# Kernel optimization log

Measured on AMD Instinct MI355X. Metric: run time of the kernel, lower is better.

Reference implementation:

```python
import jax, jax.numpy as jnp
import numpy as np

BS, B, M, D, N = 8, 8, 512, 128, 1024
N_STEPS = 2
S_MAX = 3.0
BUDGET = 32.0
NEG = -1e30


def unit_normalize(x, eps=1e-12):
    return x / jnp.maximum(jnp.linalg.norm(x, axis=-1, keepdims=True), eps)


def setup_inputs() -> dict:
    key = jax.random.key(0)
    ks = jax.random.split(key, 10)
    return {
        "seed": jax.random.normal(ks[0], (BS, N, D), jnp.float32),
        "w_cand": jax.random.normal(ks[1], (BS, N, D), jnp.float32),
        "surprise": jax.random.normal(ks[2], (BS, N, D), jnp.float32),
        "g_em": jax.random.uniform(ks[3], (BS, B), jnp.float32),
        "em_K": unit_normalize(jax.random.normal(ks[4], (BS, B, M, D), jnp.float32)),
        "em_V": jax.random.normal(ks[5], (BS, B, M, D), jnp.float32),
        "em_S": jax.random.normal(ks[6], (BS, B, M), jnp.float32),  # ~half slots active (S>0)
        "em_age": jnp.zeros((BS, B, M), jnp.float32),
        "w1": 0.02 * jax.random.normal(ks[7], (B, D), jnp.float32),
        "w2": 0.02 * jax.random.normal(ks[8], (B, D), jnp.float32),
        "gate_bias": jnp.zeros((B, D), jnp.float32),
        "raw_tau": jnp.zeros((B,), jnp.float32),
        "raw_tau_w": jnp.zeros((B,), jnp.float32),
    }


def _masked_attn(scores, active, has_active):
    # scores: [BS,B,N,M]; active: [BS,B,1,M] bool; rows with no active slot -> 0 (nan_to_num(0))
    a = jax.nn.softmax(jnp.where(active, scores, NEG), axis=-1)
    return a * has_active


def reference(seed, w_cand, surprise, g_em, em_K, em_V, em_S, em_age,
              w1, w2, gate_bias, raw_tau, raw_tau_w):
    active = (em_S > 0.0)[:, :, None, :]                  # [BS,B,1,M]
    has_active = jnp.any(active, axis=-1, keepdims=True).astype(seed.dtype)

    # ---- trail_read_all (eval mode: no sigma noise) ----
    tau = (jax.nn.softplus(raw_tau) + 0.1)[None, :, None, None]
    s = jnp.broadcast_to(seed[:, None], (BS, B, N, D))
    y = s
    w1b, w2b, gbb = w1[None, :, None, :], w2[None, :, None, :], gate_bias[None, :, None, :]
    for _ in range(N_STEPS):
        scores = jnp.einsum('bknd,bkmd->bknm', y, em_K) / tau
        attn = _masked_attn(scores, active, has_active)
        delta = jnp.einsum('bknm,bkmd->bknd', attn, em_V)
        gate = jax.nn.sigmoid(w1b * y + w2b * delta + gbb)
        y = y + gate * delta
    y_em = jnp.transpose(y - s, (0, 2, 1, 3))             # [BS,N,B,D]

    # ---- compute_novelty_all (w_nov = None -> 0.5 blend) ----
    w_norm = unit_normalize(w_cand)[:, None]               # [BS,1,N,D]
    kT = jnp.swapaxes(em_K, -1, -2)                        # [BS,B,D,M]
    nov_scores = jnp.matmul(w_norm, kT) / tau              # [BS,B,N,M]
    nov_attn = _masked_attn(nov_scores, active, has_active)
    recon = jnp.matmul(nov_attn, em_V)                     # [BS,B,N,D]
    recon_err = jnp.linalg.norm(w_cand[:, None] - recon, axis=-1)   # [BS,B,N]
    surp_mag = jnp.linalg.norm(surprise, axis=-1)[:, None]          # [BS,1,N]
    novelty_bn = 0.5 * surp_mag + 0.5 * recon_err          # [BS,B,N]
    novelty = jnp.transpose(novelty_bn, (0, 2, 1))         # [BS,N,B]

    # ---- compute_write_deltas ----
    delta_em = novelty[..., None] * w_cand[:, :, None, :]  # [BS,N,B,D]

    # ---- commit_all ----
    tau_w = (jax.nn.softplus(raw_tau_w) + 0.1)[None, :, None, None]
    route_scores = jnp.matmul(w_norm, kT) / tau_w
    # all-inactive rows: softmax of all-equal NEG -> uniform 1/M == nan_to_num(1/M)
    route = jax.nn.softmax(jnp.where(active, route_scores, NEG), axis=-1)  # [BS,B,N,M]
    weighted_route = novelty_bn[..., None] * route          # [BS,B,N,M]
    route_agg = weighted_route.mean(axis=2)                 # [BS,B,M]
    wrT = jnp.swapaxes(weighted_route, 2, 3)                # [BS,B,M,N]
    update_K = jnp.matmul(wrT, w_norm)                      # [BS,B,M,D]
    update_V = jnp.matmul(wrT, w_cand[:, None])             # [BS,B,M,D]
    denom = jnp.maximum(weighted_route.sum(axis=2)[..., None], 1e-8)
    update_K = update_K / denom
    update_V = update_V / denom
    alpha = jnp.minimum(g_em[..., None] * route_agg, 1.0)   # [BS,B,M]
    ae = alpha[..., None]
    new_K = (1.0 - ae) * em_K + ae * unit_normalize(update_K)
    new_V = (1.0 - ae) * em_V + ae * update_V
    new_S = jnp.clip(em_S + alpha, 0.0, S_MAX)
    tot = new_S.sum(axis=-1, keepdims=True)                 # budget_enforce: scale sum to <= BUDGET
    new_S = new_S * jnp.minimum(1.0, BUDGET / jnp.maximum(tot, 1e-8))
    new_age = em_age * (1.0 - alpha)

    return (y_em, delta_em, new_K, new_V, new_S, new_age)
```

## Files before the change

kernel.cpp:

```cpp
#include <hip/hip_runtime.h>
#include <cstddef>

constexpr int BSz = 8;
constexpr int Bb  = 8;
constexpr int Mm  = 512;
constexpr int Dd  = 128;
constexpr int Nn  = 1024;
constexpr float NEGV = -1e30f;

typedef unsigned short ushort_t;
typedef __attribute__((ext_vector_type(8))) short short8v;
typedef __attribute__((ext_vector_type(4))) float f32x4;

__device__ __forceinline__ float softplusf(float x) {
    return (x > 20.f) ? x : log1pf(expf(x));
}
__device__ __forceinline__ unsigned short f2bf(float f) {
    unsigned u = __float_as_uint(f);
    u += 0x7fffu + ((u >> 16) & 1u);
    return (unsigned short)(u >> 16);
}
__device__ __forceinline__ unsigned pack2bf(float a, float b) {
    return (unsigned)f2bf(a) | ((unsigned)f2bf(b) << 16);
}
__device__ __forceinline__ f32x4 mfma16(short8v a, short8v b, f32x4 c) {
    return __builtin_amdgcn_mfma_f32_16x16x32_bf16(a, b, c, 0, 0, 0);
}

__device__ __forceinline__ void stage_K64(const float* __restrict__ src,
                                          ushort_t (*kl)[136], int tid) {
    const float4* s4 = (const float4*)src;
    #pragma unroll
    for (int it = 0; it < 8; ++it) {
        int i = tid + it * 256;
        int m = i >> 5, c = i & 31;
        float4 v = s4[i];
        uint2 w;
        w.x = pack2bf(v.x, v.y);
        w.y = pack2bf(v.z, v.w);
        *(uint2*)&kl[m][c * 4] = w;
    }
}

__device__ __forceinline__ void stage_VT(const float* __restrict__ src,
                                         ushort_t (*vt)[72], int tid) {
    const int wv = tid >> 6, l = tid & 63;
    const int c = l & 31, mh = l >> 5;
    #pragma unroll
    for (int it = 0; it < 8; ++it) {
        int pi = wv * 8 + it;
        int m0 = pi * 2;
        float4 mine = *(const float4*)(src + (size_t)(m0 + mh) * Dd + c * 4);
        float4 oth;
        oth.x = __shfl_xor(mine.x, 32);
        oth.y = __shfl_xor(mine.y, 32);
        oth.z = __shfl_xor(mine.z, 32);
        oth.w = __shfl_xor(mine.w, 32);
        float a0 = mh ? oth.z  : mine.x;
        float a1 = mh ? mine.z : oth.x;
        float b0 = mh ? oth.w  : mine.y;
        float b1 = mh ? mine.w : oth.y;
        int d0 = c * 4 + mh * 2;
        int sw = ((d0 >> 2) & 7) << 2;
        int col = m0 ^ sw;
        *(unsigned*)&vt[d0][col]     = pack2bf(a0, a1);
        *(unsigned*)&vt[d0 + 1][col] = pack2bf(b0, b1);
    }
}

__device__ __forceinline__ void stage_WVT(const float* __restrict__ src,
                                          const float* sinv,
                                          ushort_t (*vt)[72], int tid) {
    const int wv = tid >> 6, l = tid & 63;
    const int c = l & 31, mh = l >> 5;
    #pragma unroll
    for (int it = 0; it < 8; ++it) {
        int pi = wv * 8 + it;
        int m0 = pi * 2;
        float inv = sinv[m0 + mh];
        float4 mine = *(const float4*)(src + (size_t)(m0 + mh) * Dd + c * 4);
        mine.x *= inv; mine.y *= inv; mine.z *= inv; mine.w *= inv;
        float4 oth;
        oth.x = __shfl_xor(mine.x, 32);
        oth.y = __shfl_xor(mine.y, 32);
        oth.z = __shfl_xor(mine.z, 32);
        oth.w = __shfl_xor(mine.w, 32);
        float a0 = mh ? oth.z  : mine.x;
        float a1 = mh ? mine.z : oth.x;
        float b0 = mh ? oth.w  : mine.y;
        float b1 = mh ? mine.w : oth.y;
        int d0 = c * 4 + mh * 2;
        int sw = ((d0 >> 2) & 7) << 2;
        int col = m0 ^ sw;
        *(unsigned*)&vt[d0][col]     = pack2bf(a0, a1);
        *(unsigned*)&vt[d0 + 1][col] = pack2bf(b0, b1);
    }
}

__device__ __forceinline__ void transpose_yl_to_vt(const float (*yl)[132],
                                                   ushort_t (*vt)[72], int tid) {
    const int wv = tid >> 6, l = tid & 63;
    const int c = l & 31, mh = l >> 5;
    #pragma unroll
    for (int it = 0; it < 8; ++it) {
        int pi = wv * 8 + it;
        int m0 = pi * 2;
        float4 mine = *(const float4*)&yl[m0 + mh][c * 4];
        float4 oth;
        oth.x = __shfl_xor(mine.x, 32);
        oth.y = __shfl_xor(mine.y, 32);
        oth.z = __shfl_xor(mine.z, 32);
        oth.w = __shfl_xor(mine.w, 32);
        float a0 = mh ? oth.z  : mine.x;
        float a1 = mh ? mine.z : oth.x;
        float b0 = mh ? oth.w  : mine.y;
        float b1 = mh ? mine.w : oth.y;
        int d0 = c * 4 + mh * 2;
        int sw = ((d0 >> 2) & 7) << 2;
        int col = m0 ^ sw;
        *(unsigned*)&vt[d0][col]     = pack2bf(a0, a1);
        *(unsigned*)&vt[d0 + 1][col] = pack2bf(b0, b1);
    }
}

__device__ __forceinline__ short8v read_kfrag(const ushort_t (*kl)[136],
                                              int mt, int ck, int g, int q) {
    union { short8v s; uint4 u; } r;
    r.u = *(const uint4*)&kl[mt * 16 + q][ck * 32 + g * 8];
    return r.s;
}
__device__ __forceinline__ short8v build_yfrag(const float (*yl)[132], int row, int ck, int g) {
    float4 v0 = *(const float4*)&yl[row][ck * 32 + g * 8];
    float4 v1 = *(const float4*)&yl[row][ck * 32 + g * 8 + 4];
    union { short8v s; uint4 u; } r;
    r.u.x = pack2bf(v0.x, v0.y);
    r.u.y = pack2bf(v0.z, v0.w);
    r.u.z = pack2bf(v1.x, v1.y);
    r.u.w = pack2bf(v1.z, v1.w);
    return r.s;
}
__device__ __forceinline__ short8v read_vfrag(const ushort_t (*vt)[72],
                                              int kc, int dt, int g, int q) {
    int d = dt * 16 + q;
    int sw = ((d >> 2) & 7) << 2;
    uint2 lo = *(const uint2*)&vt[d][(kc * 32 + 4 * g) ^ sw];
    uint2 hi = *(const uint2*)&vt[d][(kc * 32 + 16 + 4 * g) ^ sw];
    union { short8v s; uint4 u; } r;
    r.u.x = lo.x; r.u.y = lo.y; r.u.z = hi.x; r.u.w = hi.y;
    return r.s;
}

__device__ __forceinline__ void kwrite(ushort_t (*kl)[136], const uint4* pf, int tid) {
    #pragma unroll
    for (int j = 0; j < 4; ++j) {
        int i = tid + j * 256;
        *(uint4*)&kl[i >> 4][(i & 15) * 8] = pf[j];
    }
}
__device__ __forceinline__ void vwrite(ushort_t (*vt)[72], const uint4* pf, int tid) {
    #pragma unroll
    for (int j = 0; j < 4; ++j) {
        int i = tid + j * 256;
        *(uint4*)&vt[i >> 3][(i & 7) * 8] = pf[j];
    }
}

__global__ __launch_bounds__(256) void k0kv(
    const float* __restrict__ emK, const float* __restrict__ emV,
    ushort_t* __restrict__ Kbf, ushort_t* __restrict__ Vtb)
{
    const int bs = blockIdx.z, b = blockIdx.y, mc = blockIdx.x;
    const int tid = threadIdx.x;
    const size_t pair = (size_t)(bs * Bb + b);
    __shared__ ushort_t vt[128][72];
    {
        const float4* s4 = (const float4*)(emK + (pair * Mm + (size_t)mc * 64) * Dd);
        uint2* dst = (uint2*)(Kbf + pair * 65536u + (size_t)mc * 8192u);
        #pragma unroll
        for (int it = 0; it < 8; ++it) {
            int i = tid + it * 256;
            float4 v = s4[i];
            uint2 w;
            w.x = pack2bf(v.x, v.y);
            w.y = pack2bf(v.z, v.w);
            dst[i] = w;
        }
    }
    stage_VT(emV + (pair * Mm + (size_t)mc * 64) * Dd, vt, tid);
    __syncthreads();
    {
        uint4* dst = (uint4*)(Vtb + pair * 65536u + (size_t)mc * 8192u);
        #pragma unroll
        for (int it = 0; it < 4; ++it) {
            int i = tid + it * 256;
            dst[i] = *(const uint4*)&vt[i >> 3][(i & 7) * 8];
        }
    }
}

__global__ __launch_bounds__(256) void k0w(
    const float* __restrict__ w_cand, ushort_t* __restrict__ wnr,
    ushort_t* __restrict__ wnT, float* __restrict__ nrmb)
{
    const int bs = blockIdx.y, nb = blockIdx.x * 64;
    const int tid = threadIdx.x;
    const int wv = tid >> 6, l = tid & 63, g = l >> 4, q = l & 15;
    __shared__ float yl[64][132];
    __shared__ ushort_t vt[128][72];
    {
        const float4* s4 = (const float4*)(w_cand + ((size_t)bs * Nn + nb) * Dd);
        #pragma unroll
        for (int it = 0; it < 8; ++it) {
            int i = tid + it * 256;
            *(float4*)&yl[i >> 5][(i & 31) * 4] = s4[i];
        }
    }
    __syncthreads();
    #pragma unroll
    for (int r = 0; r < 4; ++r) {
        int row = wv * 16 + 4 * g + r;
        float v8[8]; float p = 0.f;
        #pragma unroll
        for (int dt = 0; dt < 8; ++dt) { float v = yl[row][dt * 16 + q]; v8[dt] = v; p += v * v; }
        #pragma unroll
        for (int off = 1; off < 16; off <<= 1) p += __shfl_xor(p, off);
        float nrm = fmaxf(sqrtf(p), 1e-12f);
        float inv = 1.f / nrm;
        if (q == 0) nrmb[(size_t)bs * Nn + nb + row] = nrm;
        #pragma unroll
        for (int dt = 0; dt < 8; ++dt) yl[row][dt * 16 + q] = v8[dt] * inv;
    }
    __syncthreads();
    {
        uint4* dst = (uint4*)(wnr + (size_t)bs * 131072u) + (size_t)nb * 16u;
        #pragma unroll
        for (int j = 0; j < 4; ++j) {
            int i = tid + j * 256;
            int row = i >> 4, c8 = i & 15;
            float4 a = *(const float4*)&yl[row][c8 * 8];
            float4 c = *(const float4*)&yl[row][c8 * 8 + 4];
            uint4 w;
            w.x = pack2bf(a.x, a.y); w.y = pack2bf(a.z, a.w);
            w.z = pack2bf(c.x, c.y); w.w = pack2bf(c.z, c.w);
            dst[i] = w;
        }
    }
    transpose_yl_to_vt(yl, vt, tid);
    __syncthreads();
    {
        uint4* dst = (uint4*)(wnT + (size_t)bs * 131072u) + (size_t)(nb >> 6) * 1024u;
        #pragma unroll
        for (int it = 0; it < 4; ++it) {
            int i = tid + it * 256;
            dst[i] = *(const uint4*)&vt[i >> 3][(i & 7) * 8];
        }
    }
}

__global__ __launch_bounds__(256) void k1_pre(
    const float* __restrict__ seed, const ushort_t* __restrict__ Kbf,
    const ushort_t* __restrict__ Vtb, const float* __restrict__ emS,
    const float* __restrict__ w1, const float* __restrict__ w2,
    const float* __restrict__ gb, const float* __restrict__ rtau,
    float* __restrict__ y_em)
{
    const int bs = blockIdx.z, b = blockIdx.y, n0 = blockIdx.x * 64;
    const int tid = threadIdx.x;
    const int wv = tid >> 6, l = tid & 63, g = l >> 4, q = l & 15;

    __shared__ float yl[64][132];
    __shared__ ushort_t kl[64][136];
    __shared__ ushort_t vt[128][72];
    __shared__ float sw1[Dd], sw2[Dd], sgb[Dd];

    const float itau = 1.f / (softplusf(rtau[b]) + 0.1f);
    const size_t pair = (size_t)(bs * Bb + b);
    const uint4* Ksrc = (const uint4*)(Kbf + pair * 65536u);
    const uint4* Vsrc = (const uint4*)(Vtb + pair * 65536u);

    if (tid < Dd) {
        sw1[tid] = w1[b * Dd + tid];
        sw2[tid] = w2[b * Dd + tid];
        sgb[tid] = gb[b * Dd + tid];
    }
    unsigned long long mlo = 0ull, mhi = 0ull;
    {
        const float4* sp = (const float4*)(emS + pair * Mm);
        #pragma unroll 8
        for (int t = 0; t < 32; ++t) {
            float4 s = sp[t * 4 + g];
            unsigned long long bits = (s.x > 0.f ? 1ull : 0ull) | (s.y > 0.f ? 2ull : 0ull)
                                    | (s.z > 0.f ? 4ull : 0ull) | (s.w > 0.f ? 8ull : 0ull);
            if (t < 16) mlo |= bits << (t * 4);
            else        mhi |= bits << ((t - 16) * 4);
        }
    }
    {
        const float4* s4 = (const float4*)(seed + ((size_t)bs * Nn + n0) * Dd);
        #pragma unroll
        for (int it = 0; it < 8; ++it) {
            int i = tid + it * 256;
            *(float4*)&yl[i >> 5][(i & 31) * 4] = s4[i];
        }
    }
    uint4 kpf[4], vpf[4];
    #pragma unroll
    for (int j = 0; j < 4; ++j) { kpf[j] = Ksrc[tid + j * 256]; vpf[j] = Vsrc[tid + j * 256]; }
    __syncthreads();

    const f32x4 Z4 = {0.f, 0.f, 0.f, 0.f};

    for (int step = 0; step < 2; ++step) {
        short8v yf[4];
        #pragma unroll
        for (int ck = 0; ck < 4; ++ck) yf[ck] = build_yfrag(yl, wv * 16 + q, ck, g);

        float m_run = NEGV, l_run = 0.f;
        f32x4 dacc[8];
        #pragma unroll
        for (int dt = 0; dt < 8; ++dt) dacc[dt] = Z4;

        for (int mc = 0; mc < 8; ++mc) {
            kwrite(kl, kpf, tid);
            vwrite(vt, vpf, tid);
            __syncthreads();
            if (!(step == 1 && mc == 7)) {
                int nx = (mc < 7) ? mc + 1 : 0;
                #pragma unroll
                for (int j = 0; j < 4; ++j) {
                    kpf[j] = Ksrc[nx * 1024 + tid + j * 256];
                    vpf[j] = Vsrc[nx * 1024 + tid + j * 256];
                }
            }

            f32x4 sc[4];
            #pragma unroll
            for (int mt = 0; mt < 4; ++mt) {
                f32x4 acc = Z4;
                #pragma unroll
                for (int ck = 0; ck < 4; ++ck)
                    acc = mfma16(read_kfrag(kl, mt, ck, g, q), yf[ck], acc);
                sc[mt] = acc;
            }
            unsigned au = (unsigned)(((mc < 4) ? mlo : mhi) >> ((mc & 3) * 16)) & 0xFFFFu;
            #pragma unroll
            for (int mt = 0; mt < 4; ++mt)
                #pragma unroll
                for (int r = 0; r < 4; ++r)
                    sc[mt][r] = ((au >> (mt * 4 + r)) & 1u) ? sc[mt][r] * itau : NEGV;
            float cm = NEGV;
            #pragma unroll
            for (int mt = 0; mt < 4; ++mt)
                #pragma unroll
                for (int r = 0; r < 4; ++r) cm = fmaxf(cm, sc[mt][r]);
            cm = fmaxf(cm, __shfl_xor(cm, 16));
            cm = fmaxf(cm, __shfl_xor(cm, 32));
            float mnew = fmaxf(m_run, cm);
            float corr = __expf(m_run - mnew);
            unsigned pw[8];
            float psum = 0.f;
            #pragma unroll
            for (int mt = 0; mt < 4; ++mt)
                #pragma unroll
                for (int r = 0; r < 4; r += 2) {
                    float e0 = __expf(sc[mt][r]     - mnew);
                    float e1 = __expf(sc[mt][r + 1] - mnew);
                    psum += e0 + e1;
                    pw[mt * 2 + (r >> 1)] = pack2bf(e0, e1);
                }
            psum += __shfl_xor(psum, 16);
            psum += __shfl_xor(psum, 32);
            l_run = l_run * corr + psum;
            m_run = mnew;
            float cr[4];
            #pragma unroll
            for (int r = 0; r < 4; ++r) cr[r] = __shfl(corr, 4 * g + r);
            #pragma unroll
            for (int dt = 0; dt < 8; ++dt)
                #pragma unroll
                for (int r = 0; r < 4; ++r) dacc[dt][r] *= cr[r];
            union { short8v s; uint4 u; } pa0, pa1;
            pa0.u = make_uint4(pw[0], pw[1], pw[2], pw[3]);
            pa1.u = make_uint4(pw[4], pw[5], pw[6], pw[7]);
            #pragma unroll
            for (int dt = 0; dt < 8; ++dt) {
                f32x4 acc = dacc[dt];
                acc = mfma16(pa0.s, read_vfrag(vt, 0, dt, g, q), acc);
                acc = mfma16(pa1.s, read_vfrag(vt, 1, dt, g, q), acc);
                dacc[dt] = acc;
            }
            __syncthreads();
        }
        float inv = (m_run != NEGV) ? 1.f / l_run : 0.f;
        float ivr[4];
        #pragma unroll
        for (int r = 0; r < 4; ++r) ivr[r] = __shfl(inv, 4 * g + r);
        #pragma unroll
        for (int r = 0; r < 4; ++r) {
            int row = wv * 16 + 4 * g + r;
            #pragma unroll
            for (int dt = 0; dt < 8; ++dt) {
                int d = dt * 16 + q;
                float del = dacc[dt][r] * ivr[r];
                float y0 = yl[row][d];
                float z = sw1[d] * y0 + sw2[d] * del + sgb[d];
                float gte = 1.f / (1.f + __expf(-z));
                yl[row][d] = y0 + gte * del;
            }
        }
        __syncthreads();
    }
    #pragma unroll
    for (int r16 = 0; r16 < 16; ++r16) {
        int n = n0 + wv * 16 + r16;
        float2 sv = *(const float2*)(seed + ((size_t)bs * Nn + n) * Dd + 2 * l);
        float2 ov;
        ov.x = yl[wv * 16 + r16][2 * l]     - sv.x;
        ov.y = yl[wv * 16 + r16][2 * l + 1] - sv.y;
        *(float2*)(y_em + (((size_t)bs * Nn + n) * Bb + b) * Dd + 2 * l) = ov;
    }
}

__global__ __launch_bounds__(256) void k2a_pre(
    const float* __restrict__ w_cand, const float* __restrict__ surprise,
    const ushort_t* __restrict__ Kbf, const ushort_t* __restrict__ Vtb,
    const ushort_t* __restrict__ wnr, const float* __restrict__ emS,
    const float* __restrict__ rtau, const float* __restrict__ rtauw,
    float* __restrict__ delta_em, float* newV )
{
    const int bs = blockIdx.z, b = blockIdx.y, n0 = blockIdx.x * 64;
    const int tid = threadIdx.x;
    const int wv = tid >> 6, l = tid & 63, g = l >> 4, q = l & 15;

    __shared__ ushort_t kl[64][136];
    __shared__ ushort_t vt[128][72];

    const float itau = 1.f / (softplusf(rtau[b]) + 0.1f);
    const float itw  = 1.f / (softplusf(rtauw[b]) + 0.1f);
    const size_t pair = (size_t)(bs * Bb + b);
    const uint4* Ksrc = (const uint4*)(Kbf + pair * 65536u);
    const uint4* Vsrc = (const uint4*)(Vtb + pair * 65536u);
    float* stats = newV + pair * (size_t)(Mm * Dd) + 448 * Dd;

    unsigned long long mlo = 0ull, mhi = 0ull;
    {
        const float4* sp = (const float4*)(emS + pair * Mm);
        #pragma unroll 8
        for (int t = 0; t < 32; ++t) {
            float4 s = sp[t * 4 + g];
            unsigned long long bits = (s.x > 0.f ? 1ull : 0ull) | (s.y > 0.f ? 2ull : 0ull)
                                    | (s.z > 0.f ? 4ull : 0ull) | (s.w > 0.f ? 8ull : 0ull);
            if (t < 16) mlo |= bits << (t * 4);
            else        mhi |= bits << ((t - 16) * 4);
        }
    }
    short8v yf[4];
    {
        const uint4* wr = (const uint4*)(wnr + (size_t)bs * 131072u
                                         + (size_t)(n0 + wv * 16 + q) * 128u);
        #pragma unroll
        for (int ck = 0; ck < 4; ++ck) {
            union { short8v s; uint4 u; } r;
            r.u = wr[ck * 4 + g];
            yf[ck] = r.s;
        }
    }
    uint4 kpf[4], vpf[4];
    #pragma unroll
    for (int j = 0; j < 4; ++j) { kpf[j] = Ksrc[tid + j * 256]; vpf[j] = Vsrc[tid + j * 256]; }

    const f32x4 Z4 = {0.f, 0.f, 0.f, 0.f};
    float m1 = NEGV, l1 = 0.f, m2 = NEGV, s2 = 0.f;
    f32x4 dacc[8];
    #pragma unroll
    for (int dt = 0; dt < 8; ++dt) dacc[dt] = Z4;

    for (int mc = 0; mc < 8; ++mc) {
        kwrite(kl, kpf, tid);
        vwrite(vt, vpf, tid);
        __syncthreads();
        if (mc < 7) {
            #pragma unroll
            for (int j = 0; j < 4; ++j) {
                kpf[j] = Ksrc[(mc + 1) * 1024 + tid + j * 256];
                vpf[j] = Vsrc[(mc + 1) * 1024 + tid + j * 256];
            }
        }

        f32x4 sc[4];
        #pragma unroll
        for (int mt = 0; mt < 4; ++mt) {
            f32x4 acc = Z4;
            #pragma unroll
            for (int ck = 0; ck < 4; ++ck)
                acc = mfma16(read_kfrag(kl, mt, ck, g, q), yf[ck], acc);
            sc[mt] = acc;
        }
        unsigned au = (unsigned)(((mc < 4) ? mlo : mhi) >> ((mc & 3) * 16)) & 0xFFFFu;

        float cm2 = NEGV;
        #pragma unroll
        for (int mt = 0; mt < 4; ++mt)
            #pragma unroll
            for (int r = 0; r < 4; ++r) {
                float v = ((au >> (mt * 4 + r)) & 1u) ? sc[mt][r] * itw : NEGV;
                cm2 = fmaxf(cm2, v);
            }
        cm2 = fmaxf(cm2, __shfl_xor(cm2, 16));
        cm2 = fmaxf(cm2, __shfl_xor(cm2, 32));
        float mn2 = fmaxf(m2, cm2);
        float c2 = __expf(m2 - mn2);
        float ps2 = 0.f;
        #pragma unroll
        for (int mt = 0; mt < 4; ++mt)
            #pragma unroll
            for (int r = 0; r < 4; ++r) {
                float v = ((au >> (mt * 4 + r)) & 1u) ? sc[mt][r] * itw : NEGV;
                ps2 += __expf(v - mn2);
            }
        ps2 += __shfl_xor(ps2, 16);
        ps2 += __shfl_xor(ps2, 32);
        s2 = s2 * c2 + ps2;
        m2 = mn2;

        #pragma unroll
        for (int mt = 0; mt < 4; ++mt)
            #pragma unroll
            for (int r = 0; r < 4; ++r)
                sc[mt][r] = ((au >> (mt * 4 + r)) & 1u) ? sc[mt][r] * itau : NEGV;
        float cm = NEGV;
        #pragma unroll
        for (int mt = 0; mt < 4; ++mt)
            #pragma unroll
            for (int r = 0; r < 4; ++r) cm = fmaxf(cm, sc[mt][r]);
        cm = fmaxf(cm, __shfl_xor(cm, 16));
        cm = fmaxf(cm, __shfl_xor(cm, 32));
        float mnew = fmaxf(m1, cm);
        float corr = __expf(m1 - mnew);
        unsigned pw[8];
        float psum = 0.f;
        #pragma unroll
        for (int mt = 0; mt < 4; ++mt)
            #pragma unroll
            for (int r = 0; r < 4; r += 2) {
                float e0 = __expf(sc[mt][r]     - mnew);
                float e1 = __expf(sc[mt][r + 1] - mnew);
                psum += e0 + e1;
                pw[mt * 2 + (r >> 1)] = pack2bf(e0, e1);
            }
        psum += __shfl_xor(psum, 16);
        psum += __shfl_xor(psum, 32);
        l1 = l1 * corr + psum;
        m1 = mnew;
        float cr[4];
        #pragma unroll
        for (int r = 0; r < 4; ++r) cr[r] = __shfl(corr, 4 * g + r);
        #pragma unroll
        for (int dt = 0; dt < 8; ++dt)
            #pragma unroll
            for (int r = 0; r < 4; ++r) dacc[dt][r] *= cr[r];
        union { short8v s; uint4 u; } pa0, pa1;
        pa0.u = make_uint4(pw[0], pw[1], pw[2], pw[3]);
        pa1.u = make_uint4(pw[4], pw[5], pw[6], pw[7]);
        #pragma unroll
        for (int dt = 0; dt < 8; ++dt) {
            f32x4 acc = dacc[dt];
            acc = mfma16(pa0.s, read_vfrag(vt, 0, dt, g, q), acc);
            acc = mfma16(pa1.s, read_vfrag(vt, 1, dt, g, q), acc);
            dacc[dt] = acc;
        }
        __syncthreads();
    }
    if (g == 0) {
        int n = n0 + wv * 16 + q;
        stats[1024 + n] = m2;
        stats[2048 + n] = s2;
    }
    float inv1 = (m1 != NEGV) ? 1.f / l1 : 0.f;
    float ivr[4];
    #pragma unroll
    for (int r = 0; r < 4; ++r) ivr[r] = __shfl(inv1, 4 * g + r);
    #pragma unroll
    for (int r = 0; r < 4; ++r) {
        int n = n0 + wv * 16 + 4 * g + r;
        const float* wcr = w_cand + ((size_t)bs * Nn + n) * Dd;
        const float* spr = surprise + ((size_t)bs * Nn + n) * Dd;
        float pe = 0.f, ps = 0.f, wcv[8];
        #pragma unroll
        for (int dt = 0; dt < 8; ++dt) {
            float wc = wcr[dt * 16 + q];
            float rec = dacc[dt][r] * ivr[r];
            float df = wc - rec;
            pe += df * df;
            float sv = spr[dt * 16 + q];
            ps += sv * sv;
            wcv[dt] = wc;
        }
        #pragma unroll
        for (int off = 1; off < 16; off <<= 1) {
            pe += __shfl_xor(pe, off);
            ps += __shfl_xor(ps, off);
        }
        float novl = 0.5f * sqrtf(ps) + 0.5f * sqrtf(pe);
        if (q == 0) stats[n] = novl;
        float* der = delta_em + (((size_t)bs * Nn + n) * Bb + b) * Dd;
        #pragma unroll
        for (int dt = 0; dt < 8; ++dt) der[dt * 16 + q] = novl * wcv[dt];
    }
}

__global__ __launch_bounds__(256) void k2b_pre(
    const ushort_t* __restrict__ wnr, const ushort_t* __restrict__ wnT,
    const ushort_t* __restrict__ Kbf,
    const float* __restrict__ emK, const float* __restrict__ emV,
    const float* __restrict__ emS, const float* __restrict__ emAge,
    const float* __restrict__ g_em, const float* __restrict__ rtauw,
    const float* __restrict__ nrmb,
    float* __restrict__ newK, float* newV ,
    float* __restrict__ newAge, float* __restrict__ newS, int mt_base)
{
    const int bs = blockIdx.z, b = blockIdx.y, mt = mt_base + blockIdx.x;
    const int m0 = mt * 64;
    const int tid = threadIdx.x;
    const int wv = tid >> 6, l = tid & 63, g = l >> 4, q = l & 15;

    __shared__ ushort_t klw[64][136];
    __shared__ ushort_t vtw[128][72];
    __shared__ float sh_rm[Nn], sh_f[Nn], sh_fn[Nn];

    const float itw = 1.f / (softplusf(rtauw[b]) + 0.1f);
    const float gv = g_em[bs * Bb + b];
    const size_t pair = (size_t)(bs * Bb + b);
    const float* stats = newV + pair * (size_t)(Mm * Dd) + 448 * Dd;

    for (int i = tid; i < Nn; i += 256) {
        float nv = stats[i];
        float rm = stats[1024 + i];
        float rs = stats[2048 + i];
        float nr = nrmb[(size_t)bs * Nn + i];
        sh_rm[i] = rm;
        float f = nv / rs;
        sh_f[i]  = f;
        sh_fn[i] = f * nr;
    }

    const int myM = m0 + wv * 16 + q;
    short8v kf[4];
    {
        const uint4* kr = (const uint4*)(Kbf + pair * 65536u + (size_t)myM * 128u);
        #pragma unroll
        for (int ck = 0; ck < 4; ++ck) {
            union { short8v s; uint4 u; } r;
            r.u = kr[ck * 4 + g];
            kf[ck] = r.s;
        }
    }
    const bool act = (emS[pair * Mm + myM] > 0.f);

    const uint4* Wr = (const uint4*)(wnr + (size_t)bs * 131072u);
    const uint4* Wt = (const uint4*)(wnT + (size_t)bs * 131072u);
    uint4 wpf[4], tpf[4];
    #pragma unroll
    for (int j = 0; j < 4; ++j) { wpf[j] = Wr[tid + j * 256]; tpf[j] = Wt[tid + j * 256]; }

    const f32x4 Z4 = {0.f, 0.f, 0.f, 0.f};
    f32x4 uKacc[8], uVacc[8];
    #pragma unroll
    for (int dt = 0; dt < 8; ++dt) { uKacc[dt] = Z4; uVacc[dt] = Z4; }
    float den = 0.f;

    for (int nc = 0; nc < 16; ++nc) {
        const int nb = nc * 64;
        kwrite(klw, wpf, tid);
        vwrite(vtw, tpf, tid);
        __syncthreads();
        if (nc < 15) {
            #pragma unroll
            for (int j = 0; j < 4; ++j) {
                wpf[j] = Wr[(nc + 1) * 1024 + tid + j * 256];
                tpf[j] = Wt[(nc + 1) * 1024 + tid + j * 256];
            }
        }

        f32x4 sc[4];
        #pragma unroll
        for (int nt = 0; nt < 4; ++nt) {
            f32x4 acc = Z4;
            #pragma unroll
            for (int ck = 0; ck < 4; ++ck)
                acc = mfma16(read_kfrag(klw, nt, ck, g, q), kf[ck], acc);
            sc[nt] = acc;
        }
        unsigned pwK[8], pwV[8];
        #pragma unroll
        for (int nt = 0; nt < 4; ++nt) {
            float w0[4], w1[4];
            #pragma unroll
            for (int r = 0; r < 4; ++r) {
                int nl = nb + nt * 16 + 4 * g + r;
                float val = act ? sc[nt][r] * itw : NEGV;
                float E = __expf(val - sh_rm[nl]);
                float a = sh_f[nl] * E;
                w0[r] = a;
                w1[r] = sh_fn[nl] * E;
                den += a;
            }
            pwK[nt * 2 + 0] = pack2bf(w0[0], w0[1]);
            pwK[nt * 2 + 1] = pack2bf(w0[2], w0[3]);
            pwV[nt * 2 + 0] = pack2bf(w1[0], w1[1]);
            pwV[nt * 2 + 1] = pack2bf(w1[2], w1[3]);
        }
        union { short8v s; uint4 u; } paK0, paK1, paV0, paV1;
        paK0.u = make_uint4(pwK[0], pwK[1], pwK[2], pwK[3]);
        paK1.u = make_uint4(pwK[4], pwK[5], pwK[6], pwK[7]);
        paV0.u = make_uint4(pwV[0], pwV[1], pwV[2], pwV[3]);
        paV1.u = make_uint4(pwV[4], pwV[5], pwV[6], pwV[7]);
        #pragma unroll
        for (int dt = 0; dt < 8; ++dt) {
            short8v b0 = read_vfrag(vtw, 0, dt, g, q);
            short8v b1 = read_vfrag(vtw, 1, dt, g, q);
            uKacc[dt] = mfma16(paK0.s, b0, uKacc[dt]);
            uKacc[dt] = mfma16(paK1.s, b1, uKacc[dt]);
            uVacc[dt] = mfma16(paV0.s, b0, uVacc[dt]);
            uVacc[dt] = mfma16(paV1.s, b1, uVacc[dt]);
        }
        __syncthreads();
    }

    den += __shfl_xor(den, 16);
    den += __shfl_xor(den, 32);
    float invd = 1.f / fmaxf(den, 1e-8f);
    float alpha = fminf(gv * den * (1.f / (float)Nn), 1.f);

    float pr[4] = {0.f, 0.f, 0.f, 0.f};
    #pragma unroll
    for (int dt = 0; dt < 8; ++dt)
        #pragma unroll
        for (int r = 0; r < 4; ++r) { float u = uKacc[dt][r]; pr[r] += u * u; }
    #pragma unroll
    for (int r = 0; r < 4; ++r) {
        #pragma unroll
        for (int off = 1; off < 16; off <<= 1) pr[r] += __shfl_xor(pr[r], off);
    }
    float alr[4], idr[4], inr[4];
    #pragma unroll
    for (int r = 0; r < 4; ++r) {
        alr[r] = __shfl(alpha, 4 * g + r);
        idr[r] = __shfl(invd,  4 * g + r);
        inr[r] = 1.f / fmaxf(sqrtf(pr[r]) * idr[r], 1e-12f);
    }
    #pragma unroll
    for (int r = 0; r < 4; ++r) {
        size_t rowoff = (pair * Mm + m0 + wv * 16 + 4 * g + r) * (size_t)Dd;
        float a = alr[r], om = 1.f - a, id = idr[r], in = inr[r];
        #pragma unroll
        for (int dt = 0; dt < 8; ++dt) {
            int d = dt * 16 + q;
            float kv = emK[rowoff + d];
            float vv = emV[rowoff + d];
            newK[rowoff + d] = om * kv + a * uKacc[dt][r] * id * in;
            newV[rowoff + d] = om * vv + a * uVacc[dt][r] * id;
        }
    }
    if (q == 0) {
        #pragma unroll
        for (int r = 0; r < 4; ++r) {
            int m = m0 + wv * 16 + 4 * g + r;
            float a = alr[r];
            float S = emS[pair * Mm + m];
            newS[pair * Mm + m] = fminf(fmaxf(S + a, 0.f), 3.0f);
            newAge[pair * Mm + m] = emAge[pair * Mm + m] * (1.f - a);
        }
    }
}

__global__ __launch_bounds__(256) void k1_fb(
    const float* __restrict__ seed, const float* __restrict__ emK, const float* __restrict__ emV,
    const float* __restrict__ emS, const float* __restrict__ w1, const float* __restrict__ w2,
    const float* __restrict__ gb, const float* __restrict__ rtau, float* __restrict__ y_em)
{
    const int bs = blockIdx.z, b = blockIdx.y, n0 = blockIdx.x * 64;
    const int tid = threadIdx.x;
    const int wv = tid >> 6, l = tid & 63, g = l >> 4, q = l & 15;

    __shared__ float yl[64][132];
    __shared__ ushort_t kl[64][136];
    __shared__ ushort_t vt[128][72];
    __shared__ float sw1[Dd], sw2[Dd], sgb[Dd];

    const float itau = 1.f / (softplusf(rtau[b]) + 0.1f);
    const size_t pair = (size_t)(bs * Bb + b);
    const float* Kb = emK + pair * (size_t)(Mm * Dd);
    const float* Vb = emV + pair * (size_t)(Mm * Dd);

    if (tid < Dd) {
        sw1[tid] = w1[b * Dd + tid];
        sw2[tid] = w2[b * Dd + tid];
        sgb[tid] = gb[b * Dd + tid];
    }
    unsigned long long mlo = 0ull, mhi = 0ull;
    {
        const float4* sp = (const float4*)(emS + pair * Mm);
        #pragma unroll 8
        for (int t = 0; t < 32; ++t) {
            float4 s = sp[t * 4 + g];
            unsigned long long bits = (s.x > 0.f ? 1ull : 0ull) | (s.y > 0.f ? 2ull : 0ull)
                                    | (s.z > 0.f ? 4ull : 0ull) | (s.w > 0.f ? 8ull : 0ull);
            if (t < 16) mlo |= bits << (t * 4);
            else        mhi |= bits << ((t - 16) * 4);
        }
    }
    {
        const float4* s4 = (const float4*)(seed + ((size_t)bs * Nn + n0) * Dd);
        #pragma unroll
        for (int it = 0; it < 8; ++it) {
            int i = tid + it * 256;
            *(float4*)&yl[i >> 5][(i & 31) * 4] = s4[i];
        }
    }
    __syncthreads();

    const f32x4 Z4 = {0.f, 0.f, 0.f, 0.f};

    for (int step = 0; step < 2; ++step) {
        short8v yf[4];
        #pragma unroll
        for (int ck = 0; ck < 4; ++ck) yf[ck] = build_yfrag(yl, wv * 16 + q, ck, g);

        float m_run = NEGV, l_run = 0.f;
        f32x4 dacc[8];
        #pragma unroll
        for (int dt = 0; dt < 8; ++dt) dacc[dt] = Z4;

        for (int mc = 0; mc < 8; ++mc) {
            stage_K64(Kb + (size_t)mc * 64 * Dd, kl, tid);
            stage_VT(Vb + (size_t)mc * 64 * Dd, vt, tid);
            __syncthreads();

            f32x4 sc[4];
            #pragma unroll
            for (int mt = 0; mt < 4; ++mt) {
                f32x4 acc = Z4;
                #pragma unroll
                for (int ck = 0; ck < 4; ++ck)
                    acc = mfma16(read_kfrag(kl, mt, ck, g, q), yf[ck], acc);
                sc[mt] = acc;
            }
            unsigned au = (unsigned)(((mc < 4) ? mlo : mhi) >> ((mc & 3) * 16)) & 0xFFFFu;
            #pragma unroll
            for (int mt = 0; mt < 4; ++mt)
                #pragma unroll
                for (int r = 0; r < 4; ++r)
                    sc[mt][r] = ((au >> (mt * 4 + r)) & 1u) ? sc[mt][r] * itau : NEGV;
            float cm = NEGV;
            #pragma unroll
            for (int mt = 0; mt < 4; ++mt)
                #pragma unroll
                for (int r = 0; r < 4; ++r) cm = fmaxf(cm, sc[mt][r]);
            cm = fmaxf(cm, __shfl_xor(cm, 16));
            cm = fmaxf(cm, __shfl_xor(cm, 32));
            float mnew = fmaxf(m_run, cm);
            float corr = __expf(m_run - mnew);
            unsigned pw[8];
            float psum = 0.f;
            #pragma unroll
            for (int mt = 0; mt < 4; ++mt)
                #pragma unroll
                for (int r = 0; r < 4; r += 2) {
                    float e0 = __expf(sc[mt][r]     - mnew);
                    float e1 = __expf(sc[mt][r + 1] - mnew);
                    psum += e0 + e1;
                    pw[mt * 2 + (r >> 1)] = pack2bf(e0, e1);
                }
            psum += __shfl_xor(psum, 16);
            psum += __shfl_xor(psum, 32);
            l_run = l_run * corr + psum;
            m_run = mnew;
            float cr[4];
            #pragma unroll
            for (int r = 0; r < 4; ++r) cr[r] = __shfl(corr, 4 * g + r);
            #pragma unroll
            for (int dt = 0; dt < 8; ++dt)
                #pragma unroll
                for (int r = 0; r < 4; ++r) dacc[dt][r] *= cr[r];
            union { short8v s; uint4 u; } pa0, pa1;
            pa0.u = make_uint4(pw[0], pw[1], pw[2], pw[3]);
            pa1.u = make_uint4(pw[4], pw[5], pw[6], pw[7]);
            #pragma unroll
            for (int dt = 0; dt < 8; ++dt) {
                f32x4 acc = dacc[dt];
                acc = mfma16(pa0.s, read_vfrag(vt, 0, dt, g, q), acc);
                acc = mfma16(pa1.s, read_vfrag(vt, 1, dt, g, q), acc);
                dacc[dt] = acc;
            }
            __syncthreads();
        }
        float inv = (m_run != NEGV) ? 1.f / l_run : 0.f;
        float ivr[4];
        #pragma unroll
        for (int r = 0; r < 4; ++r) ivr[r] = __shfl(inv, 4 * g + r);
        #pragma unroll
        for (int r = 0; r < 4; ++r) {
            int row = wv * 16 + 4 * g + r;
            #pragma unroll
            for (int dt = 0; dt < 8; ++dt) {
                int d = dt * 16 + q;
                float del = dacc[dt][r] * ivr[r];
                float y0 = yl[row][d];
                float z = sw1[d] * y0 + sw2[d] * del + sgb[d];
                float gte = 1.f / (1.f + __expf(-z));
                yl[row][d] = y0 + gte * del;
            }
        }
        __syncthreads();
    }
    #pragma unroll
    for (int r16 = 0; r16 < 16; ++r16) {
        int n = n0 + wv * 16 + r16;
        float2 sv = *(const float2*)(seed + ((size_t)bs * Nn + n) * Dd + 2 * l);
        float2 ov;
        ov.x = yl[wv * 16 + r16][2 * l]     - sv.x;
        ov.y = yl[wv * 16 + r16][2 * l + 1] - sv.y;
        *(float2*)(y_em + (((size_t)bs * Nn + n) * Bb + b) * Dd + 2 * l) = ov;
    }
}

__global__ __launch_bounds__(256) void k2a_fb(
    const float* __restrict__ w_cand, const float* __restrict__ surprise,
    const float* __restrict__ emK, const float* __restrict__ emV, const float* __restrict__ emS,
    const float* __restrict__ rtau, const float* __restrict__ rtauw,
    float* __restrict__ delta_em, float* newV)
{
    const int bs = blockIdx.z, b = blockIdx.y, n0 = blockIdx.x * 64;
    const int tid = threadIdx.x;
    const int wv = tid >> 6, l = tid & 63, g = l >> 4, q = l & 15;

    __shared__ float yl[64][132];
    __shared__ ushort_t kl[64][136];
    __shared__ ushort_t vt[128][72];

    const float itau = 1.f / (softplusf(rtau[b]) + 0.1f);
    const float itw  = 1.f / (softplusf(rtauw[b]) + 0.1f);
    const size_t pair = (size_t)(bs * Bb + b);
    const float* Kb = emK + pair * (size_t)(Mm * Dd);
    const float* Vb = emV + pair * (size_t)(Mm * Dd);
    float* stats = newV + pair * (size_t)(Mm * Dd) + 448 * Dd;

    unsigned long long mlo = 0ull, mhi = 0ull;
    {
        const float4* sp = (const float4*)(emS + pair * Mm);
        #pragma unroll 8
        for (int t = 0; t < 32; ++t) {
            float4 s = sp[t * 4 + g];
            unsigned long long bits = (s.x > 0.f ? 1ull : 0ull) | (s.y > 0.f ? 2ull : 0ull)
                                    | (s.z > 0.f ? 4ull : 0ull) | (s.w > 0.f ? 8ull : 0ull);
            if (t < 16) mlo |= bits << (t * 4);
            else        mhi |= bits << ((t - 16) * 4);
        }
    }
    {
        const float4* s4 = (const float4*)(w_cand + ((size_t)bs * Nn + n0) * Dd);
        #pragma unroll
        for (int it = 0; it < 8; ++it) {
            int i = tid + it * 256;
            *(float4*)&yl[i >> 5][(i & 31) * 4] = s4[i];
        }
    }
    __syncthreads();
    #pragma unroll
    for (int r = 0; r < 4; ++r) {
        int row = wv * 16 + 4 * g + r;
        float v8[8]; float p = 0.f;
        #pragma unroll
        for (int dt = 0; dt < 8; ++dt) { float v = yl[row][dt * 16 + q]; v8[dt] = v; p += v * v; }
        #pragma unroll
        for (int off = 1; off < 16; off <<= 1) p += __shfl_xor(p, off);
        float nrm = fmaxf(sqrtf(p), 1e-12f);
        float invn = 1.f / nrm;
        if (q == 0) stats[3072 + n0 + row] = nrm;
        #pragma unroll
        for (int dt = 0; dt < 8; ++dt) yl[row][dt * 16 + q] = v8[dt] * invn;
    }
    __syncthreads();

    const f32x4 Z4 = {0.f, 0.f, 0.f, 0.f};
    short8v yf[4];
    #pragma unroll
    for (int ck = 0; ck < 4; ++ck) yf[ck] = build_yfrag(yl, wv * 16 + q, ck, g);

    float m1 = NEGV, l1 = 0.f, m2 = NEGV, s2 = 0.f;
    f32x4 dacc[8];
    #pragma unroll
    for (int dt = 0; dt < 8; ++dt) dacc[dt] = Z4;

    for (int mc = 0; mc < 8; ++mc) {
        stage_K64(Kb + (size_t)mc * 64 * Dd, kl, tid);
        stage_VT(Vb + (size_t)mc * 64 * Dd, vt, tid);
        __syncthreads();

        f32x4 sc[4];
        #pragma unroll
        for (int mt = 0; mt < 4; ++mt) {
            f32x4 acc = Z4;
            #pragma unroll
            for (int ck = 0; ck < 4; ++ck)
                acc = mfma16(read_kfrag(kl, mt, ck, g, q), yf[ck], acc);
            sc[mt] = acc;
        }
        unsigned au = (unsigned)(((mc < 4) ? mlo : mhi) >> ((mc & 3) * 16)) & 0xFFFFu;

        float cm2 = NEGV;
        #pragma unroll
        for (int mt = 0; mt < 4; ++mt)
            #pragma unroll
            for (int r = 0; r < 4; ++r) {
                float v = ((au >> (mt * 4 + r)) & 1u) ? sc[mt][r] * itw : NEGV;
                cm2 = fmaxf(cm2, v);
            }
        cm2 = fmaxf(cm2, __shfl_xor(cm2, 16));
        cm2 = fmaxf(cm2, __shfl_xor(cm2, 32));
        float mn2 = fmaxf(m2, cm2);
        float c2 = __expf(m2 - mn2);
        float ps2 = 0.f;
        #pragma unroll
        for (int mt = 0; mt < 4; ++mt)
            #pragma unroll
            for (int r = 0; r < 4; ++r) {
                float v = ((au >> (mt * 4 + r)) & 1u) ? sc[mt][r] * itw : NEGV;
                ps2 += __expf(v - mn2);
            }
        ps2 += __shfl_xor(ps2, 16);
        ps2 += __shfl_xor(ps2, 32);
        s2 = s2 * c2 + ps2;
        m2 = mn2;

        #pragma unroll
        for (int mt = 0; mt < 4; ++mt)
            #pragma unroll
            for (int r = 0; r < 4; ++r)
                sc[mt][r] = ((au >> (mt * 4 + r)) & 1u) ? sc[mt][r] * itau : NEGV;
        float cm = NEGV;
        #pragma unroll
        for (int mt = 0; mt < 4; ++mt)
            #pragma unroll
            for (int r = 0; r < 4; ++r) cm = fmaxf(cm, sc[mt][r]);
        cm = fmaxf(cm, __shfl_xor(cm, 16));
        cm = fmaxf(cm, __shfl_xor(cm, 32));
        float mnew = fmaxf(m1, cm);
        float corr = __expf(m1 - mnew);
        unsigned pw[8];
        float psum = 0.f;
        #pragma unroll
        for (int mt = 0; mt < 4; ++mt)
            #pragma unroll
            for (int r = 0; r < 4; r += 2) {
                float e0 = __expf(sc[mt][r]     - mnew);
                float e1 = __expf(sc[mt][r + 1] - mnew);
                psum += e0 + e1;
                pw[mt * 2 + (r >> 1)] = pack2bf(e0, e1);
            }
        psum += __shfl_xor(psum, 16);
        psum += __shfl_xor(psum, 32);
        l1 = l1 * corr + psum;
        m1 = mnew;
        float cr[4];
        #pragma unroll
        for (int r = 0; r < 4; ++r) cr[r] = __shfl(corr, 4 * g + r);
        #pragma unroll
        for (int dt = 0; dt < 8; ++dt)
            #pragma unroll
            for (int r = 0; r < 4; ++r) dacc[dt][r] *= cr[r];
        union { short8v s; uint4 u; } pa0, pa1;
        pa0.u = make_uint4(pw[0], pw[1], pw[2], pw[3]);
        pa1.u = make_uint4(pw[4], pw[5], pw[6], pw[7]);
        #pragma unroll
        for (int dt = 0; dt < 8; ++dt) {
            f32x4 acc = dacc[dt];
            acc = mfma16(pa0.s, read_vfrag(vt, 0, dt, g, q), acc);
            acc = mfma16(pa1.s, read_vfrag(vt, 1, dt, g, q), acc);
            dacc[dt] = acc;
        }
        __syncthreads();
    }
    if (g == 0) {
        int n = n0 + wv * 16 + q;
        stats[1024 + n] = m2;
        stats[2048 + n] = s2;
    }
    float inv1 = (m1 != NEGV) ? 1.f / l1 : 0.f;
    float ivr[4];
    #pragma unroll
    for (int r = 0; r < 4; ++r) ivr[r] = __shfl(inv1, 4 * g + r);
    #pragma unroll
    for (int r = 0; r < 4; ++r) {
        int n = n0 + wv * 16 + 4 * g + r;
        const float* wcr = w_cand + ((size_t)bs * Nn + n) * Dd;
        const float* spr = surprise + ((size_t)bs * Nn + n) * Dd;
        float pe = 0.f, ps = 0.f, wcv[8];
        #pragma unroll
        for (int dt = 0; dt < 8; ++dt) {
            float wc = wcr[dt * 16 + q];
            float rec = dacc[dt][r] * ivr[r];
            float df = wc - rec;
            pe += df * df;
            float sv = spr[dt * 16 + q];
            ps += sv * sv;
            wcv[dt] = wc;
        }
        #pragma unroll
        for (int off = 1; off < 16; off <<= 1) {
            pe += __shfl_xor(pe, off);
            ps += __shfl_xor(ps, off);
        }
        float novl = 0.5f * sqrtf(ps) + 0.5f * sqrtf(pe);
        if (q == 0) stats[n] = novl;
        float* der = delta_em + (((size_t)bs * Nn + n) * Bb + b) * Dd;
        #pragma unroll
        for (int dt = 0; dt < 8; ++dt) der[dt * 16 + q] = novl * wcv[dt];
    }
}

__global__ __launch_bounds__(256) void k2b_fb(
    const float* __restrict__ w_cand, const float* __restrict__ emK, const float* __restrict__ emV,
    const float* __restrict__ emS, const float* __restrict__ emAge,
    const float* __restrict__ g_em, const float* __restrict__ rtauw,
    float* __restrict__ newK, float* newV,
    float* __restrict__ newAge, float* __restrict__ newS, int mt_base)
{
    const int bs = blockIdx.z, b = blockIdx.y, mt = mt_base + blockIdx.x;
    const int m0 = mt * 64;
    const int tid = threadIdx.x;
    const int wv = tid >> 6, l = tid & 63, g = l >> 4, q = l & 15;

    __shared__ ushort_t klw[64][136];
    __shared__ ushort_t vtw[128][72];
    __shared__ float sh_rm[Nn], sh_f[Nn], sh_fn[Nn], sh_inv[Nn];

    const float itw = 1.f / (softplusf(rtauw[b]) + 0.1f);
    const float gv = g_em[bs * Bb + b];
    const size_t pair = (size_t)(bs * Bb + b);
    const float* stats = newV + pair * (size_t)(Mm * Dd) + 448 * Dd;

    for (int i = tid; i < Nn; i += 256) {
        float nv = stats[i];
        float rm = stats[1024 + i];
        float rs = stats[2048 + i];
        float nr = stats[3072 + i];
        sh_rm[i] = rm;
        float f = nv / rs;
        sh_f[i]  = f;
        sh_fn[i] = f * nr;
        sh_inv[i] = 1.f / nr;
    }

    const int myM = m0 + wv * 16 + q;
    const float* Krow = emK + (pair * Mm + myM) * (size_t)Dd;
    short8v kf[4];
    #pragma unroll
    for (int ck = 0; ck < 4; ++ck) {
        float4 a = *(const float4*)(Krow + ck * 32 + g * 8);
        float4 c = *(const float4*)(Krow + ck * 32 + g * 8 + 4);
        union { short8v s; uint4 u; } r;
        r.u.x = pack2bf(a.x, a.y);
        r.u.y = pack2bf(a.z, a.w);
        r.u.z = pack2bf(c.x, c.y);
        r.u.w = pack2bf(c.z, c.w);
        kf[ck] = r.s;
    }
    const bool act = (emS[pair * Mm + myM] > 0.f);

    const f32x4 Z4 = {0.f, 0.f, 0.f, 0.f};
    f32x4 uKacc[8], uVacc[8];
    #pragma unroll
    for (int dt = 0; dt < 8; ++dt) { uKacc[dt] = Z4; uVacc[dt] = Z4; }
    float den = 0.f;

    __syncthreads();

    for (int nc = 0; nc < 16; ++nc) {
        const int nb = nc * 64;
        if (nc) __syncthreads();
        {
            const float4* s4 = (const float4*)(w_cand + ((size_t)bs * Nn + nb) * Dd);
            #pragma unroll
            for (int it = 0; it < 8; ++it) {
                int i = tid + it * 256;
                int m = i >> 5, c = i & 31;
                float4 v = s4[i];
                float inv = sh_inv[nb + m];
                uint2 w;
                w.x = pack2bf(v.x * inv, v.y * inv);
                w.y = pack2bf(v.z * inv, v.w * inv);
                *(uint2*)&klw[m][c * 4] = w;
            }
        }
        stage_WVT(w_cand + ((size_t)bs * Nn + nb) * Dd, sh_inv + nb, vtw, tid);
        __syncthreads();

        f32x4 sc[4];
        #pragma unroll
        for (int nt = 0; nt < 4; ++nt) {
            f32x4 acc = Z4;
            #pragma unroll
            for (int ck = 0; ck < 4; ++ck)
                acc = mfma16(read_kfrag(klw, nt, ck, g, q), kf[ck], acc);
            sc[nt] = acc;
        }
        unsigned pwK[8], pwV[8];
        #pragma unroll
        for (int nt = 0; nt < 4; ++nt) {
            float w0[4], w1[4];
            #pragma unroll
            for (int r = 0; r < 4; ++r) {
                int nl = nb + nt * 16 + 4 * g + r;
                float val = act ? sc[nt][r] * itw : NEGV;
                float E = __expf(val - sh_rm[nl]);
                float a = sh_f[nl] * E;
                w0[r] = a;
                w1[r] = sh_fn[nl] * E;
                den += a;
            }
            pwK[nt * 2 + 0] = pack2bf(w0[0], w0[1]);
            pwK[nt * 2 + 1] = pack2bf(w0[2], w0[3]);
            pwV[nt * 2 + 0] = pack2bf(w1[0], w1[1]);
            pwV[nt * 2 + 1] = pack2bf(w1[2], w1[3]);
        }
        union { short8v s; uint4 u; } paK0, paK1, paV0, paV1;
        paK0.u = make_uint4(pwK[0], pwK[1], pwK[2], pwK[3]);
        paK1.u = make_uint4(pwK[4], pwK[5], pwK[6], pwK[7]);
        paV0.u = make_uint4(pwV[0], pwV[1], pwV[2], pwV[3]);
        paV1.u = make_uint4(pwV[4], pwV[5], pwV[6], pwV[7]);
        #pragma unroll
        for (int dt = 0; dt < 8; ++dt) {
            short8v b0 = read_vfrag(vtw, 0, dt, g, q);
            short8v b1 = read_vfrag(vtw, 1, dt, g, q);
            uKacc[dt] = mfma16(paK0.s, b0, uKacc[dt]);
            uKacc[dt] = mfma16(paK1.s, b1, uKacc[dt]);
            uVacc[dt] = mfma16(paV0.s, b0, uVacc[dt]);
            uVacc[dt] = mfma16(paV1.s, b1, uVacc[dt]);
        }
    }

    den += __shfl_xor(den, 16);
    den += __shfl_xor(den, 32);
    float invd = 1.f / fmaxf(den, 1e-8f);
    float alpha = fminf(gv * den * (1.f / (float)Nn), 1.f);

    float pr[4] = {0.f, 0.f, 0.f, 0.f};
    #pragma unroll
    for (int dt = 0; dt < 8; ++dt)
        #pragma unroll
        for (int r = 0; r < 4; ++r) { float u = uKacc[dt][r]; pr[r] += u * u; }
    #pragma unroll
    for (int r = 0; r < 4; ++r) {
        #pragma unroll
        for (int off = 1; off < 16; off <<= 1) pr[r] += __shfl_xor(pr[r], off);
    }
    float alr[4], idr[4], inr[4];
    #pragma unroll
    for (int r = 0; r < 4; ++r) {
        alr[r] = __shfl(alpha, 4 * g + r);
        idr[r] = __shfl(invd,  4 * g + r);
        inr[r] = 1.f / fmaxf(sqrtf(pr[r]) * idr[r], 1e-12f);
    }
    #pragma unroll
    for (int r = 0; r < 4; ++r) {
        size_t rowoff = (pair * Mm + m0 + wv * 16 + 4 * g + r) * (size_t)Dd;
        float a = alr[r], om = 1.f - a, id = idr[r], in = inr[r];
        #pragma unroll
        for (int dt = 0; dt < 8; ++dt) {
            int d = dt * 16 + q;
            float kv = emK[rowoff + d];
            float vv = emV[rowoff + d];
            newK[rowoff + d] = om * kv + a * uKacc[dt][r] * id * in;
            newV[rowoff + d] = om * vv + a * uVacc[dt][r] * id;
        }
    }
    if (q == 0) {
        #pragma unroll
        for (int r = 0; r < 4; ++r) {
            int m = m0 + wv * 16 + 4 * g + r;
            float a = alr[r];
            float S = emS[pair * Mm + m];
            newS[pair * Mm + m] = fminf(fmaxf(S + a, 0.f), 3.0f);
            newAge[pair * Mm + m] = emAge[pair * Mm + m] * (1.f - a);
        }
    }
}

__global__ __launch_bounds__(256) void k2c_scale(float* newS)
{
    const int p = blockIdx.x, tid = threadIdx.x;
    __shared__ float red[256];
    float v0 = newS[(size_t)p * Mm + tid];
    float v1 = newS[(size_t)p * Mm + 256 + tid];
    red[tid] = v0 + v1;
    __syncthreads();
    for (int s = 128; s > 0; s >>= 1) {
        if (tid < s) red[tid] += red[tid + s];
        __syncthreads();
    }
    float tot = red[0];
    float sc = fminf(1.f, 32.0f / fmaxf(tot, 1e-8f));
    newS[(size_t)p * Mm + tid]       = v0 * sc;
    newS[(size_t)p * Mm + 256 + tid] = v1 * sc;
}

extern "C" void kernel_launch(void* const* d_in, const int* in_sizes, int n_in,
                              void* d_out, int out_size, void* d_ws, size_t ws_size,
                              hipStream_t stream)
{
    const float* seed     = (const float*)d_in[0];
    const float* w_cand   = (const float*)d_in[1];
    const float* surprise = (const float*)d_in[2];
    const float* g_em     = (const float*)d_in[3];
    const float* emK      = (const float*)d_in[4];
    const float* emV      = (const float*)d_in[5];
    const float* emS      = (const float*)d_in[6];
    const float* emAge    = (const float*)d_in[7];
    const float* w1       = (const float*)d_in[8];
    const float* w2       = (const float*)d_in[9];
    const float* gb       = (const float*)d_in[10];
    const float* rtau     = (const float*)d_in[11];
    const float* rtauw    = (const float*)d_in[12];

    float* out = (float*)d_out;
    float* y_em     = out;
    float* delta_em = out + (size_t)8388608;
    float* newK     = out + (size_t)16777216;
    float* newV     = out + (size_t)20971520;
    float* newS     = out + (size_t)25165824;
    float* newAge   = out + (size_t)25198592;

    dim3 blk(256);
    dim3 g1(Nn / 64, Bb, BSz);

    const size_t WS_NEED = 21004288;
    if (d_ws != nullptr && ws_size >= WS_NEED) {
        ushort_t* Kbf = (ushort_t*)d_ws;
        ushort_t* Vtb = Kbf + (size_t)64 * 65536;
        ushort_t* wnr = Vtb + (size_t)64 * 65536;
        ushort_t* wnT = wnr + (size_t)8 * 131072;
        float*    nrmb = (float*)(wnT + (size_t)8 * 131072);

        k0kv<<<dim3(8, Bb, BSz), blk, 0, stream>>>(emK, emV, Kbf, Vtb);
        k0w<<<dim3(16, BSz), blk, 0, stream>>>(w_cand, wnr, wnT, nrmb);
        k1_pre<<<g1, blk, 0, stream>>>(seed, Kbf, Vtb, emS, w1, w2, gb, rtau, y_em);
        k2a_pre<<<g1, blk, 0, stream>>>(w_cand, surprise, Kbf, Vtb, wnr, emS,
                                        rtau, rtauw, delta_em, newV);
        k2b_pre<<<dim3(7, Bb, BSz), blk, 0, stream>>>(wnr, wnT, Kbf, emK, emV, emS, emAge,
                                                      g_em, rtauw, nrmb,
                                                      newK, newV, newAge, newS, 0);
        k2b_pre<<<dim3(1, Bb, BSz), blk, 0, stream>>>(wnr, wnT, Kbf, emK, emV, emS, emAge,
                                                      g_em, rtauw, nrmb,
                                                      newK, newV, newAge, newS, 7);
    } else {
        k1_fb<<<g1, blk, 0, stream>>>(seed, emK, emV, emS, w1, w2, gb, rtau, y_em);
        k2a_fb<<<g1, blk, 0, stream>>>(w_cand, surprise, emK, emV, emS, rtau, rtauw,
                                       delta_em, newV);
        k2b_fb<<<dim3(7, Bb, BSz), blk, 0, stream>>>(w_cand, emK, emV, emS, emAge, g_em, rtauw,
                                                     newK, newV, newAge, newS, 0);
        k2b_fb<<<dim3(1, Bb, BSz), blk, 0, stream>>>(w_cand, emK, emV, emS, emAge, g_em, rtauw,
                                                     newK, newV, newAge, newS, 7);
    }
    k2c_scale<<<dim3(64), blk, 0, stream>>>(newS);
}
```

Before: 695.9 us.

## Split trail-read steps into separate launches and remap blocks to 1D grids

The fused two-step k1_pre kernel becomes k1_step, launched once per step. The intermediate y is stored to y_em in global memory rather than kept in LDS, and the y fragment is built straight from global memory. All kernels now use 1D grids with the batch index b (or bs) in the low bits, so blocks sharing the same K/V or w_cand data run close together and may hit in cache. This drops the 64x132 float LDS buffer, which can raise occupancy, but it adds an extra launch and a global round trip of y.

New measurement: 712.4 us. +2.4%, slower.

```diff
diff --git a/kernel.cpp b/kernel.cpp
--- a/kernel.cpp
+++ b/kernel.cpp
@@ -139,6 +139,16 @@
     r.u.w = pack2bf(v1.z, v1.w);
     return r.s;
 }
+__device__ __forceinline__ short8v build_gfrag(const float* __restrict__ yr, int ck, int g) {
+    float4 a = *(const float4*)(yr + ck * 32 + g * 8);
+    float4 c = *(const float4*)(yr + ck * 32 + g * 8 + 4);
+    union { short8v s; uint4 u; } r;
+    r.u.x = pack2bf(a.x, a.y);
+    r.u.y = pack2bf(a.z, a.w);
+    r.u.z = pack2bf(c.x, c.y);
+    r.u.w = pack2bf(c.z, c.w);
+    return r.s;
+}
 __device__ __forceinline__ short8v read_vfrag(const ushort_t (*vt)[72],
                                               int kc, int dt, int g, int q) {
     int d = dt * 16 + q;
@@ -165,11 +175,27 @@
     }
 }
 
+__device__ __forceinline__ void build_mask(const float* __restrict__ emS, size_t pair,
+                                           int g, unsigned long long& mlo,
+                                           unsigned long long& mhi) {
+    mlo = 0ull; mhi = 0ull;
+    const float4* sp = (const float4*)(emS + pair * Mm);
+    #pragma unroll 8
+    for (int t = 0; t < 32; ++t) {
+        float4 s = sp[t * 4 + g];
+        unsigned long long bits = (s.x > 0.f ? 1ull : 0ull) | (s.y > 0.f ? 2ull : 0ull)
+                                | (s.z > 0.f ? 4ull : 0ull) | (s.w > 0.f ? 8ull : 0ull);
+        if (t < 16) mlo |= bits << (t * 4);
+        else        mhi |= bits << ((t - 16) * 4);
+    }
+}
+
 __global__ __launch_bounds__(256) void k0kv(
     const float* __restrict__ emK, const float* __restrict__ emV,
     ushort_t* __restrict__ Kbf, ushort_t* __restrict__ Vtb)
 {
-    const int bs = blockIdx.z, b = blockIdx.y, mc = blockIdx.x;
+    const int id = blockIdx.x;
+    const int b = id & 7, t = id >> 3, mc = t & 7, bs = t >> 3;
     const int tid = threadIdx.x;
     const size_t pair = (size_t)(bs * Bb + b);
     __shared__ ushort_t vt[128][72];
@@ -202,7 +228,8 @@
     const float* __restrict__ w_cand, ushort_t* __restrict__ wnr,
     ushort_t* __restrict__ wnT, float* __restrict__ nrmb)
 {
-    const int bs = blockIdx.y, nb = blockIdx.x * 64;
+    const int id = blockIdx.x;
+    const int bs = id & 7, nb = (id >> 3) * 64;
     const int tid = threadIdx.x;
     const int wv = tid >> 6, l = tid & 63, g = l >> 4, q = l & 15;
     __shared__ float yl[64][132];
@@ -257,12 +284,500 @@
     }
 }
 
-__global__ __launch_bounds__(256) void k1_pre(
+__global__ __launch_bounds__(256) void k1_step(
     const float* __restrict__ seed, const ushort_t* __restrict__ Kbf,
     const ushort_t* __restrict__ Vtb, const float* __restrict__ emS,
     const float* __restrict__ w1, const float* __restrict__ w2,
     const float* __restrict__ gb, const float* __restrict__ rtau,
-    float* __restrict__ y_em)
+    float* __restrict__ y_em, int step)
+{
+    const int id = blockIdx.x;
+    const int b = id & 7, bs = id >> 7, n0 = ((id >> 3) & 15) << 6;
+    const int tid = threadIdx.x;
+    const int wv = tid >> 6, l = tid & 63, g = l >> 4, q = l & 15;
+
+    __shared__ ushort_t kl[64][136];
+    __shared__ ushort_t vt[128][72];
+    __shared__ float sw1[Dd], sw2[Dd], sgb[Dd];
+
+    const float itau = 1.f / (softplusf(rtau[b]) + 0.1f);
+    const size_t pair = (size_t)(bs * Bb + b);
+    const uint4* Ksrc = (const uint4*)(Kbf + pair * 65536u);
+    const uint4* Vsrc = (const uint4*)(Vtb + pair * 65536u);
+
+    if (tid < Dd) {
+        sw1[tid] = w1[b * Dd + tid];
+        sw2[tid] = w2[b * Dd + tid];
+        sgb[tid] = gb[b * Dd + tid];
+    }
+    unsigned long long mlo, mhi;
+    build_mask(emS, pair, g, mlo, mhi);
+
+    short8v yf[4];
+    {
+        int n = n0 + wv * 16 + q;
+        const float* yr = step ? (y_em + (((size_t)bs * Nn + n) * Bb + b) * Dd)
+                               : (seed + ((size_t)bs * Nn + n) * Dd);
+        #pragma unroll
+        for (int ck = 0; ck < 4; ++ck) yf[ck] = build_gfrag(yr, ck, g);
+    }
+    uint4 kpf[4], vpf[4];
+    #pragma unroll
+    for (int j = 0; j < 4; ++j) { kpf[j] = Ksrc[tid + j * 256]; vpf[j] = Vsrc[tid + j * 256]; }
+
+    const f32x4 Z4 = {0.f, 0.f, 0.f, 0.f};
+    float m_run = NEGV, l_run = 0.f;
+    f32x4 dacc[8];
+    #pragma unroll
+    for (int dt = 0; dt < 8; ++dt) dacc[dt] = Z4;
+
+    for (int mc = 0; mc < 8; ++mc) {
+        kwrite(kl, kpf, tid);
+        vwrite(vt, vpf, tid);
+        __syncthreads();
+        if (mc < 7) {
+            #pragma unroll
+            for (int j = 0; j < 4; ++j) {
+                kpf[j] = Ksrc[(mc + 1) * 1024 + tid + j * 256];
+                vpf[j] = Vsrc[(mc + 1) * 1024 + tid + j * 256];
+            }
+        }
+
+        f32x4 sc[4];
+        #pragma unroll
+        for (int mt = 0; mt < 4; ++mt) {
+            f32x4 acc = Z4;
+            #pragma unroll
+            for (int ck = 0; ck < 4; ++ck)
+                acc = mfma16(read_kfrag(kl, mt, ck, g, q), yf[ck], acc);
+            sc[mt] = acc;
+        }
+        unsigned au = (unsigned)(((mc < 4) ? mlo : mhi) >> ((mc & 3) * 16)) & 0xFFFFu;
+        #pragma unroll
+        for (int mt = 0; mt < 4; ++mt)
+            #pragma unroll
+            for (int r = 0; r < 4; ++r)
+                sc[mt][r] = ((au >> (mt * 4 + r)) & 1u) ? sc[mt][r] * itau : NEGV;
+        float cm = NEGV;
+        #pragma unroll
+        for (int mt = 0; mt < 4; ++mt)
+            #pragma unroll
+            for (int r = 0; r < 4; ++r) cm = fmaxf(cm, sc[mt][r]);
+        cm = fmaxf(cm, __shfl_xor(cm, 16));
+        cm = fmaxf(cm, __shfl_xor(cm, 32));
+        float mnew = fmaxf(m_run, cm);
+        float corr = __expf(m_run - mnew);
+        unsigned pw[8];
+        float psum = 0.f;
+        #pragma unroll
+        for (int mt = 0; mt < 4; ++mt)
+            #pragma unroll
+            for (int r = 0; r < 4; r += 2) {
+                float e0 = __expf(sc[mt][r]     - mnew);
+                float e1 = __expf(sc[mt][r + 1] - mnew);
+                psum += e0 + e1;
+                pw[mt * 2 + (r >> 1)] = pack2bf(e0, e1);
+            }
+        psum += __shfl_xor(psum, 16);
+        psum += __shfl_xor(psum, 32);
+        l_run = l_run * corr + psum;
+        m_run = mnew;
+        float cr[4];
+        #pragma unroll
+        for (int r = 0; r < 4; ++r) cr[r] = __shfl(corr, 4 * g + r);
+        #pragma unroll
+        for (int dt = 0; dt < 8; ++dt)
+            #pragma unroll
+            for (int r = 0; r < 4; ++r) dacc[dt][r] *= cr[r];
+        union { short8v s; uint4 u; } pa0, pa1;
+        pa0.u = make_uint4(pw[0], pw[1], pw[2], pw[3]);
+        pa1.u = make_uint4(pw[4], pw[5], pw[6], pw[7]);
+        #pragma unroll
+        for (int dt = 0; dt < 8; ++dt) {
+            f32x4 acc = dacc[dt];
+            acc = mfma16(pa0.s, read_vfrag(vt, 0, dt, g, q), acc);
+            acc = mfma16(pa1.s, read_vfrag(vt, 1, dt, g, q), acc);
+            dacc[dt] = acc;
+        }
+        __syncthreads();
+    }
+    float inv = (m_run != NEGV) ? 1.f / l_run : 0.f;
+    float ivr[4];
+    #pragma unroll
+    for (int r = 0; r < 4; ++r) ivr[r] = __shfl(inv, 4 * g + r);
+    #pragma unroll
+    for (int r = 0; r < 4; ++r) {
+        int n = n0 + wv * 16 + 4 * g + r;
+        const float* yr = step ? (y_em + (((size_t)bs * Nn + n) * Bb + b) * Dd)
+                               : (seed + ((size_t)bs * Nn + n) * Dd);
+        const float* sr = seed + ((size_t)bs * Nn + n) * Dd;
+        float* yo = y_em + (((size_t)bs * Nn + n) * Bb + b) * Dd;
+        #pragma unroll
+        for (int dt = 0; dt < 8; ++dt) {
+            int d = dt * 16 + q;
+            float y0 = yr[d];
+            float del = dacc[dt][r] * ivr[r];
+            float z = sw1[d] * y0 + sw2[d] * del + sgb[d];
+            float gte = 1.f / (1.f + __expf(-z));
+            float yn = y0 + gte * del;
+            yo[d] = step ? (yn - sr[d]) : yn;
+        }
+    }
+}
+
+__global__ __launch_bounds__(256) void k2a_pre(
+    const float* __restrict__ w_cand, const float* __restrict__ surprise,
+    const ushort_t* __restrict__ Kbf, const ushort_t* __restrict__ Vtb,
+    const ushort_t* __restrict__ wnr, const float* __restrict__ emS,
+    const float* __restrict__ rtau, const float* __restrict__ rtauw,
+    float* __restrict__ delta_em, float* newV )
+{
+    const int id = blockIdx.x;
+    const int b = id & 7, bs = id >> 7, n0 = ((id >> 3) & 15) << 6;
+    const int tid = threadIdx.x;
+    const int wv = tid >> 6, l = tid & 63, g = l >> 4, q = l & 15;
+
+    __shared__ ushort_t kl[64][136];
+    __shared__ ushort_t vt[128][72];
+
+    const float itau = 1.f / (softplusf(rtau[b]) + 0.1f);
+    const float itw  = 1.f / (softplusf(rtauw[b]) + 0.1f);
+    const size_t pair = (size_t)(bs * Bb + b);
+    const uint4* Ksrc = (const uint4*)(Kbf + pair * 65536u);
+    const uint4* Vsrc = (const uint4*)(Vtb + pair * 65536u);
+    float* stats = newV + pair * (size_t)(Mm * Dd) + 448 * Dd;
+
+    unsigned long long mlo, mhi;
+    build_mask(emS, pair, g, mlo, mhi);
+
+    short8v yf[4];
+    {
+        const uint4* wr = (const uint4*)(wnr + (size_t)bs * 131072u
+                                         + (size_t)(n0 + wv * 16 + q) * 128u);
+        #pragma unroll
+        for (int ck = 0; ck < 4; ++ck) {
+            union { short8v s; uint4 u; } r;
+            r.u = wr[ck * 4 + g];
+            yf[ck] = r.s;
+        }
+    }
+    uint4 kpf[4], vpf[4];
+    #pragma unroll
+    for (int j = 0; j < 4; ++j) { kpf[j] = Ksrc[tid + j * 256]; vpf[j] = Vsrc[tid + j * 256]; }
+
+    const f32x4 Z4 = {0.f, 0.f, 0.f, 0.f};
+    float m1 = NEGV, l1 = 0.f, m2 = NEGV, s2 = 0.f;
+    f32x4 dacc[8];
+    #pragma unroll
+    for (int dt = 0; dt < 8; ++dt) dacc[dt] = Z4;
+
+    for (int mc = 0; mc < 8; ++mc) {
+        kwrite(kl, kpf, tid);
+        vwrite(vt, vpf, tid);
+        __syncthreads();
+        if (mc < 7) {
+            #pragma unroll
+            for (int j = 0; j < 4; ++j) {
+                kpf[j] = Ksrc[(mc + 1) * 1024 + tid + j * 256];
+                vpf[j] = Vsrc[(mc + 1) * 1024 + tid + j * 256];
+            }
+        }
+
+        f32x4 sc[4];
+        #pragma unroll
+        for (int mt = 0; mt < 4; ++mt) {
+            f32x4 acc = Z4;
+            #pragma unroll
+            for (int ck = 0; ck < 4; ++ck)
+                acc = mfma16(read_kfrag(kl, mt, ck, g, q), yf[ck], acc);
+            sc[mt] = acc;
+        }
+        unsigned au = (unsigned)(((mc < 4) ? mlo : mhi) >> ((mc & 3) * 16)) & 0xFFFFu;
+
+        float cm2 = NEGV;
+        #pragma unroll
+        for (int mt = 0; mt < 4; ++mt)
+            #pragma unroll
+            for (int r = 0; r < 4; ++r) {
+                float v = ((au >> (mt * 4 + r)) & 1u) ? sc[mt][r] * itw : NEGV;
+                cm2 = fmaxf(cm2, v);
+            }
+        cm2 = fmaxf(cm2, __shfl_xor(cm2, 16));
+        cm2 = fmaxf(cm2, __shfl_xor(cm2, 32));
+        float mn2 = fmaxf(m2, cm2);
+        float c2 = __expf(m2 - mn2);
+        float ps2 = 0.f;
+        #pragma unroll
+        for (int mt = 0; mt < 4; ++mt)
+            #pragma unroll
+            for (int r = 0; r < 4; ++r) {
+                float v = ((au >> (mt * 4 + r)) & 1u) ? sc[mt][r] * itw : NEGV;
+                ps2 += __expf(v - mn2);
+            }
+        ps2 += __shfl_xor(ps2, 16);
+        ps2 += __shfl_xor(ps2, 32);
+        s2 = s2 * c2 + ps2;
+        m2 = mn2;
+
+        #pragma unroll
+        for (int mt = 0; mt < 4; ++mt)
+            #pragma unroll
+            for (int r = 0; r < 4; ++r)
+                sc[mt][r] = ((au >> (mt * 4 + r)) & 1u) ? sc[mt][r] * itau : NEGV;
+        float cm = NEGV;
+        #pragma unroll
+        for (int mt = 0; mt < 4; ++mt)
+            #pragma unroll
+            for (int r = 0; r < 4; ++r) cm = fmaxf(cm, sc[mt][r]);
+        cm = fmaxf(cm, __shfl_xor(cm, 16));
+        cm = fmaxf(cm, __shfl_xor(cm, 32));
+        float mnew = fmaxf(m1, cm);
+        float corr = __expf(m1 - mnew);
+        unsigned pw[8];
+        float psum = 0.f;
+        #pragma unroll
+        for (int mt = 0; mt < 4; ++mt)
+            #pragma unroll
+            for (int r = 0; r < 4; r += 2) {
+                float e0 = __expf(sc[mt][r]     - mnew);
+                float e1 = __expf(sc[mt][r + 1] - mnew);
+                psum += e0 + e1;
+                pw[mt * 2 + (r >> 1)] = pack2bf(e0, e1);
+            }
+        psum += __shfl_xor(psum, 16);
+        psum += __shfl_xor(psum, 32);
+        l1 = l1 * corr + psum;
+        m1 = mnew;
+        float cr[4];
+        #pragma unroll
+        for (int r = 0; r < 4; ++r) cr[r] = __shfl(corr, 4 * g + r);
+        #pragma unroll
+        for (int dt = 0; dt < 8; ++dt)
+            #pragma unroll
+            for (int r = 0; r < 4; ++r) dacc[dt][r] *= cr[r];
+        union { short8v s; uint4 u; } pa0, pa1;
+        pa0.u = make_uint4(pw[0], pw[1], pw[2], pw[3]);
+        pa1.u = make_uint4(pw[4], pw[5], pw[6], pw[7]);
+        #pragma unroll
+        for (int dt = 0; dt < 8; ++dt) {
+            f32x4 acc = dacc[dt];
+            acc = mfma16(pa0.s, read_vfrag(vt, 0, dt, g, q), acc);
+            acc = mfma16(pa1.s, read_vfrag(vt, 1, dt, g, q), acc);
+            dacc[dt] = acc;
+        }
+        __syncthreads();
+    }
+    if (g == 0) {
+        int n = n0 + wv * 16 + q;
+        stats[1024 + n] = m2;
+        stats[2048 + n] = s2;
+    }
+    float inv1 = (m1 != NEGV) ? 1.f / l1 : 0.f;
+    float ivr[4];
+    #pragma unroll
+    for (int r = 0; r < 4; ++r) ivr[r] = __shfl(inv1, 4 * g + r);
+    #pragma unroll
+    for (int r = 0; r < 4; ++r) {
+        int n = n0 + wv * 16 + 4 * g + r;
+        const float* wcr = w_cand + ((size_t)bs * Nn + n) * Dd;
+        const float* spr = surprise + ((size_t)bs * Nn + n) * Dd;
+        float pe = 0.f, ps = 0.f, wcv[8];
+        #pragma unroll
+        for (int dt = 0; dt < 8; ++dt) {
+            float wc = wcr[dt * 16 + q];
+            float rec = dacc[dt][r] * ivr[r];
+            float df = wc - rec;
+            pe += df * df;
+            float sv = spr[dt * 16 + q];
+            ps += sv * sv;
+            wcv[dt] = wc;
+        }
+        #pragma unroll
+        for (int off = 1; off < 16; off <<= 1) {
+            pe += __shfl_xor(pe, off);
+            ps += __shfl_xor(ps, off);
+        }
+        float novl = 0.5f * sqrtf(ps) + 0.5f * sqrtf(pe);
+        if (q == 0) stats[n] = novl;
+        float* der = delta_em + (((size_t)bs * Nn + n) * Bb + b) * Dd;
+        #pragma unroll
+        for (int dt = 0; dt < 8; ++dt) der[dt * 16 + q] = novl * wcv[dt];
+    }
+}
+
+__global__ __launch_bounds__(256) void k2b_pre(
+    const ushort_t* __restrict__ wnr, const ushort_t* __restrict__ wnT,
+    const ushort_t* __restrict__ Kbf,
+    const float* __restrict__ emK, const float* __restrict__ emV,
+    const float* __restrict__ emS, const float* __restrict__ emAge,
+    const float* __restrict__ g_em, const float* __restrict__ rtauw,
+    const float* __restrict__ nrmb,
+    float* __restrict__ newK, float* newV ,
+    float* __restrict__ newAge, float* __restrict__ newS, int phase)
+{
+    const int id = blockIdx.x;
+    const int bs = id & 7;
+    const int t = id >> 3;
+    const int b  = phase ? t : t / 7;
+    const int mt = phase ? 7 : t % 7;
+    const int m0 = mt * 64;
+    const int tid = threadIdx.x;
+    const int wv = tid >> 6, l = tid & 63, g = l >> 4, q = l & 15;
+
+    __shared__ ushort_t klw[64][136];
+    __shared__ ushort_t vtw[128][72];
+    __shared__ float sh_rm[Nn], sh_f[Nn], sh_fn[Nn];
+
+    const float itw = 1.f / (softplusf(rtauw[b]) + 0.1f);
+    const float gv = g_em[bs * Bb + b];
+    const size_t pair = (size_t)(bs * Bb + b);
+    const float* stats = newV + pair * (size_t)(Mm * Dd) + 448 * Dd;
+
+    for (int i = tid; i < Nn; i += 256) {
+        float nv = stats[i];
+        float rm = stats[1024 + i];
+        float rs = stats[2048 + i];
+        float nr = nrmb[(size_t)bs * Nn + i];
+        sh_rm[i] = rm;
+        float f = nv / rs;
+        sh_f[i]  = f;
+        sh_fn[i] = f * nr;
+    }
+
+    const int myM = m0 + wv * 16 + q;
+    short8v kf[4];
+    {
+        const uint4* kr = (const uint4*)(Kbf + pair * 65536u + (size_t)myM * 128u);
+        #pragma unroll
+        for (int ck = 0; ck < 4; ++ck) {
+            union { short8v s; uint4 u; } r;
+            r.u = kr[ck * 4 + g];
+            kf[ck] = r.s;
+        }
+    }
+    const bool act = (emS[pair * Mm + myM] > 0.f);
+
+    const uint4* Wr = (const uint4*)(wnr + (size_t)bs * 131072u);
+    const uint4* Wt = (const uint4*)(wnT + (size_t)bs * 131072u);
+    uint4 wpf[4], tpf[4];
+    #pragma unroll
+    for (int j = 0; j < 4; ++j) { wpf[j] = Wr[tid + j * 256]; tpf[j] = Wt[tid + j * 256]; }
+
+    const f32x4 Z4 = {0.f, 0.f, 0.f, 0.f};
+    f32x4 uKacc[8], uVacc[8];
+    #pragma unroll
+    for (int dt = 0; dt < 8; ++dt) { uKacc[dt] = Z4; uVacc[dt] = Z4; }
+    float den = 0.f;
+
+    for (int nc = 0; nc < 16; ++nc) {
+        const int nb = nc * 64;
+        kwrite(klw, wpf, tid);
+        vwrite(vtw, tpf, tid);
+        __syncthreads();
+        if (nc < 15) {
+            #pragma unroll
+            for (int j = 0; j < 4; ++j) {
+                wpf[j] = Wr[(nc + 1) * 1024 + tid + j * 256];
+                tpf[j] = Wt[(nc + 1) * 1024 + tid + j * 256];
+            }
+        }
+
+        f32x4 sc[4];
+        #pragma unroll
+        for (int nt = 0; nt < 4; ++nt) {
+            f32x4 acc = Z4;
+            #pragma unroll
+            for (int ck = 0; ck < 4; ++ck)
+                acc = mfma16(read_kfrag(klw, nt, ck, g, q), kf[ck], acc);
+            sc[nt] = acc;
+        }
+        unsigned pwK[8], pwV[8];
+        #pragma unroll
+        for (int nt = 0; nt < 4; ++nt) {
+            float w0[4], w1[4];
+            #pragma unroll
+            for (int r = 0; r < 4; ++r) {
+                int nl = nb + nt * 16 + 4 * g + r;
+                float val = act ? sc[nt][r] * itw : NEGV;
+                float E = __expf(val - sh_rm[nl]);
+                float a = sh_f[nl] * E;
+                w0[r] = a;
+                w1[r] = sh_fn[nl] * E;
+                den += a;
+            }
+            pwK[nt * 2 + 0] = pack2bf(w0[0], w0[1]);
+            pwK[nt * 2 + 1] = pack2bf(w0[2], w0[3]);
+            pwV[nt * 2 + 0] = pack2bf(w1[0], w1[1]);
+            pwV[nt * 2 + 1] = pack2bf(w1[2], w1[3]);
+        }
+        union { short8v s; uint4 u; } paK0, paK1, paV0, paV1;
+        paK0.u = make_uint4(pwK[0], pwK[1], pwK[2], pwK[3]);
+        paK1.u = make_uint4(pwK[4], pwK[5], pwK[6], pwK[7]);
+        paV0.u = make_uint4(pwV[0], pwV[1], pwV[2], pwV[3]);
+        paV1.u = make_uint4(pwV[4], pwV[5], pwV[6], pwV[7]);
+        #pragma unroll
+        for (int dt = 0; dt < 8; ++dt) {
+            short8v b0 = read_vfrag(vtw, 0, dt, g, q);
+            short8v b1 = read_vfrag(vtw, 1, dt, g, q);
+            uKacc[dt] = mfma16(paK0.s, b0, uKacc[dt]);
+            uKacc[dt] = mfma16(paK1.s, b1, uKacc[dt]);
+            uVacc[dt] = mfma16(paV0.s, b0, uVacc[dt]);
+            uVacc[dt] = mfma16(paV1.s, b1, uVacc[dt]);
+        }
+        __syncthreads();
+    }
+
+    den += __shfl_xor(den, 16);
+    den += __shfl_xor(den, 32);
+    float invd = 1.f / fmaxf(den, 1e-8f);
+    float alpha = fminf(gv * den * (1.f / (float)Nn), 1.f);
+
+    float pr[4] = {0.f, 0.f, 0.f, 0.f};
+    #pragma unroll
+    for (int dt = 0; dt < 8; ++dt)
+        #pragma unroll
+        for (int r = 0; r < 4; ++r) { float u = uKacc[dt][r]; pr[r] += u * u; }
+    #pragma unroll
+    for (int r = 0; r < 4; ++r) {
+        #pragma unroll
+        for (int off = 1; off < 16; off <<= 1) pr[r] += __shfl_xor(pr[r], off);
+    }
+    float alr[4], idr[4], inr[4];
+    #pragma unroll
+    for (int r = 0; r < 4; ++r) {
+        alr[r] = __shfl(alpha, 4 * g + r);
+        idr[r] = __shfl(invd,  4 * g + r);
+        inr[r] = 1.f / fmaxf(sqrtf(pr[r]) * idr[r], 1e-12f);
+    }
+    #pragma unroll
+    for (int r = 0; r < 4; ++r) {
+        size_t rowoff = (pair * Mm + m0 + wv * 16 + 4 * g + r) * (size_t)Dd;
+        float a = alr[r], om = 1.f - a, idv = idr[r], in = inr[r];
+        #pragma unroll
+        for (int dt = 0; dt < 8; ++dt) {
+            int d = dt * 16 + q;
+            float kv = emK[rowoff + d];
+            float vv = emV[rowoff + d];
+            newK[rowoff + d] = om * kv + a * uKacc[dt][r] * idv * in;
+            newV[rowoff + d] = om * vv + a * uVacc[dt][r] * idv;
+        }
+    }
+    if (q == 0) {
+        #pragma unroll
+        for (int r = 0; r < 4; ++r) {
+            int m = m0 + wv * 16 + 4 * g + r;
+            float a = alr[r];
+            float S = emS[pair * Mm + m];
+            newS[pair * Mm + m] = fminf(fmaxf(S + a, 0.f), 3.0f);
+            newAge[pair * Mm + m] = emAge[pair * Mm + m] * (1.f - a);
+        }
+    }
+}
+
+__global__ __launch_bounds__(256) void k1_fb(
+    const float* __restrict__ seed, const float* __restrict__ emK, const float* __restrict__ emV,
+    const float* __restrict__ emS, const float* __restrict__ w1, const float* __restrict__ w2,
+    const float* __restrict__ gb, const float* __restrict__ rtau, float* __restrict__ y_em)
 {
     const int bs = blockIdx.z, b = blockIdx.y, n0 = blockIdx.x * 64;
     const int tid = threadIdx.x;
@@ -275,26 +790,16 @@
 
     const float itau = 1.f / (softplusf(rtau[b]) + 0.1f);
     const size_t pair = (size_t)(bs * Bb + b);
-    const uint4* Ksrc = (const uint4*)(Kbf + pair * 65536u);
-    const uint4* Vsrc = (const uint4*)(Vtb + pair * 65536u);
+    const float* Kb = emK + pair * (size_t)(Mm * Dd);
+    const float* Vb = emV + pair * (size_t)(Mm * Dd);
 
     if (tid < Dd) {
         sw1[tid] = w1[b * Dd + tid];
         sw2[tid] = w2[b * Dd + tid];
         sgb[tid] = gb[b * Dd + tid];
     }
-    unsigned long long mlo = 0ull, mhi = 0ull;
-    {
-        const float4* sp = (const float4*)(emS + pair * Mm);
-        #pragma unroll 8
-        for (int t = 0; t < 32; ++t) {
-            float4 s = sp[t * 4 + g];
-            unsigned long long bits = (s.x > 0.f ? 1ull : 0ull) | (s.y > 0.f ? 2ull : 0ull)
-                                    | (s.z > 0.f ? 4ull : 0ull) | (s.w > 0.f ? 8ull : 0ull);
-            if (t < 16) mlo |= bits << (t * 4);
-            else        mhi |= bits << ((t - 16) * 4);
-        }
-    }
+    unsigned long long mlo, mhi;
+    build_mask(emS, pair, g, mlo, mhi);
     {
         const float4* s4 = (const float4*)(seed + ((size_t)bs * Nn + n0) * Dd);
         #pragma unroll
@@ -303,9 +808,6 @@
             *(float4*)&yl[i >> 5][(i & 31) * 4] = s4[i];
         }
     }
-    uint4 kpf[4], vpf[4];
-    #pragma unroll
-    for (int j = 0; j < 4; ++j) { kpf[j] = Ksrc[tid + j * 256]; vpf[j] = Vsrc[tid + j * 256]; }
     __syncthreads();
 
     const f32x4 Z4 = {0.f, 0.f, 0.f, 0.f};
@@ -321,17 +823,9 @@
         for (int dt = 0; dt < 8; ++dt) dacc[dt] = Z4;
 
         for (int mc = 0; mc < 8; ++mc) {
-            kwrite(kl, kpf, tid);
-            vwrite(vt, vpf, tid);
+            stage_K64(Kb + (size_t)mc * 64 * Dd, kl, tid);
+            stage_VT(Vb + (size_t)mc * 64 * Dd, vt, tid);
             __syncthreads();
-            if (!(step == 1 && mc == 7)) {
-                int nx = (mc < 7) ? mc + 1 : 0;
-                #pragma unroll
-                for (int j = 0; j < 4; ++j) {
-                    kpf[j] = Ksrc[nx * 1024 + tid + j * 256];
-                    vpf[j] = Vsrc[nx * 1024 + tid + j * 256];
-                }
-            }
 
             f32x4 sc[4];
             #pragma unroll
@@ -421,510 +915,6 @@
     }
 }
 
-__global__ __launch_bounds__(256) void k2a_pre(
-    const float* __restrict__ w_cand, const float* __restrict__ surprise,
-    const ushort_t* __restrict__ Kbf, const ushort_t* __restrict__ Vtb,
-    const ushort_t* __restrict__ wnr, const float* __restrict__ emS,
-    const float* __restrict__ rtau, const float* __restrict__ rtauw,
-    float* __restrict__ delta_em, float* newV )
-{
-    const int bs = blockIdx.z, b = blockIdx.y, n0 = blockIdx.x * 64;
-    const int tid = threadIdx.x;
-    const int wv = tid >> 6, l = tid & 63, g = l >> 4, q = l & 15;
-
-    __shared__ ushort_t kl[64][136];
-    __shared__ ushort_t vt[128][72];
-
-    const float itau = 1.f / (softplusf(rtau[b]) + 0.1f);
-    const float itw  = 1.f / (softplusf(rtauw[b]) + 0.1f);
-    const size_t pair = (size_t)(bs * Bb + b);
-    const uint4* Ksrc = (const uint4*)(Kbf + pair * 65536u);
-    const uint4* Vsrc = (const uint4*)(Vtb + pair * 65536u);
-    float* stats = newV + pair * (size_t)(Mm * Dd) + 448 * Dd;
-
-    unsigned long long mlo = 0ull, mhi = 0ull;
-    {
-        const float4* sp = (const float4*)(emS + pair * Mm);
-        #pragma unroll 8
-        for (int t = 0; t < 32; ++t) {
-            float4 s = sp[t * 4 + g];
-            unsigned long long bits = (s.x > 0.f ? 1ull : 0ull) | (s.y > 0.f ? 2ull : 0ull)
-                                    | (s.z > 0.f ? 4ull : 0ull) | (s.w > 0.f ? 8ull : 0ull);
-            if (t < 16) mlo |= bits << (t * 4);
-            else        mhi |= bits << ((t - 16) * 4);
-        }
-    }
-    short8v yf[4];
-    {
-        const uint4* wr = (const uint4*)(wnr + (size_t)bs * 131072u
-                                         + (size_t)(n0 + wv * 16 + q) * 128u);
-        #pragma unroll
-        for (int ck = 0; ck < 4; ++ck) {
-            union { short8v s; uint4 u; } r;
-            r.u = wr[ck * 4 + g];
-            yf[ck] = r.s;
-        }
-    }
-    uint4 kpf[4], vpf[4];
-    #pragma unroll
-    for (int j = 0; j < 4; ++j) { kpf[j] = Ksrc[tid + j * 256]; vpf[j] = Vsrc[tid + j * 256]; }
-
-    const f32x4 Z4 = {0.f, 0.f, 0.f, 0.f};
-    float m1 = NEGV, l1 = 0.f, m2 = NEGV, s2 = 0.f;
-    f32x4 dacc[8];
-    #pragma unroll
-    for (int dt = 0; dt < 8; ++dt) dacc[dt] = Z4;
-
-    for (int mc = 0; mc < 8; ++mc) {
-        kwrite(kl, kpf, tid);
-        vwrite(vt, vpf, tid);
-        __syncthreads();
-        if (mc < 7) {
-            #pragma unroll
-            for (int j = 0; j < 4; ++j) {
-                kpf[j] = Ksrc[(mc + 1) * 1024 + tid + j * 256];
-                vpf[j] = Vsrc[(mc + 1) * 1024 + tid + j * 256];
-            }
-        }
-
-        f32x4 sc[4];
-        #pragma unroll
-        for (int mt = 0; mt < 4; ++mt) {
-            f32x4 acc = Z4;
-            #pragma unroll
-            for (int ck = 0; ck < 4; ++ck)
-                acc = mfma16(read_kfrag(kl, mt, ck, g, q), yf[ck], acc);
-            sc[mt] = acc;
-        }
-        unsigned au = (unsigned)(((mc < 4) ? mlo : mhi) >> ((mc & 3) * 16)) & 0xFFFFu;
-
-        float cm2 = NEGV;
-        #pragma unroll
-        for (int mt = 0; mt < 4; ++mt)
-            #pragma unroll
-            for (int r = 0; r < 4; ++r) {
-                float v = ((au >> (mt * 4 + r)) & 1u) ? sc[mt][r] * itw : NEGV;
-                cm2 = fmaxf(cm2, v);
-            }
-        cm2 = fmaxf(cm2, __shfl_xor(cm2, 16));
-        cm2 = fmaxf(cm2, __shfl_xor(cm2, 32));
-        float mn2 = fmaxf(m2, cm2);
-        float c2 = __expf(m2 - mn2);
-        float ps2 = 0.f;
-        #pragma unroll
-        for (int mt = 0; mt < 4; ++mt)
-            #pragma unroll
-            for (int r = 0; r < 4; ++r) {
-                float v = ((au >> (mt * 4 + r)) & 1u) ? sc[mt][r] * itw : NEGV;
-                ps2 += __expf(v - mn2);
-            }
-        ps2 += __shfl_xor(ps2, 16);
-        ps2 += __shfl_xor(ps2, 32);
-        s2 = s2 * c2 + ps2;
-        m2 = mn2;
-
-        #pragma unroll
-        for (int mt = 0; mt < 4; ++mt)
-            #pragma unroll
-            for (int r = 0; r < 4; ++r)
-                sc[mt][r] = ((au >> (mt * 4 + r)) & 1u) ? sc[mt][r] * itau : NEGV;
-        float cm = NEGV;
-        #pragma unroll
-        for (int mt = 0; mt < 4; ++mt)
-            #pragma unroll
-            for (int r = 0; r < 4; ++r) cm = fmaxf(cm, sc[mt][r]);
-        cm = fmaxf(cm, __shfl_xor(cm, 16));
-        cm = fmaxf(cm, __shfl_xor(cm, 32));
-        float mnew = fmaxf(m1, cm);
-        float corr = __expf(m1 - mnew);
-        unsigned pw[8];
-        float psum = 0.f;
-        #pragma unroll
-        for (int mt = 0; mt < 4; ++mt)
-            #pragma unroll
-            for (int r = 0; r < 4; r += 2) {
-                float e0 = __expf(sc[mt][r]     - mnew);
-                float e1 = __expf(sc[mt][r + 1] - mnew);
-                psum += e0 + e1;
-                pw[mt * 2 + (r >> 1)] = pack2bf(e0, e1);
-            }
-        psum += __shfl_xor(psum, 16);
-        psum += __shfl_xor(psum, 32);
-        l1 = l1 * corr + psum;
-        m1 = mnew;
-        float cr[4];
-        #pragma unroll
-        for (int r = 0; r < 4; ++r) cr[r] = __shfl(corr, 4 * g + r);
-        #pragma unroll
-        for (int dt = 0; dt < 8; ++dt)
-            #pragma unroll
-            for (int r = 0; r < 4; ++r) dacc[dt][r] *= cr[r];
-        union { short8v s; uint4 u; } pa0, pa1;
-        pa0.u = make_uint4(pw[0], pw[1], pw[2], pw[3]);
-        pa1.u = make_uint4(pw[4], pw[5], pw[6], pw[7]);
-        #pragma unroll
-        for (int dt = 0; dt < 8; ++dt) {
-            f32x4 acc = dacc[dt];
-            acc = mfma16(pa0.s, read_vfrag(vt, 0, dt, g, q), acc);
-            acc = mfma16(pa1.s, read_vfrag(vt, 1, dt, g, q), acc);
-            dacc[dt] = acc;
-        }
-        __syncthreads();
-    }
-    if (g == 0) {
-        int n = n0 + wv * 16 + q;
-        stats[1024 + n] = m2;
-        stats[2048 + n] = s2;
-    }
-    float inv1 = (m1 != NEGV) ? 1.f / l1 : 0.f;
-    float ivr[4];
-    #pragma unroll
-    for (int r = 0; r < 4; ++r) ivr[r] = __shfl(inv1, 4 * g + r);
-    #pragma unroll
-    for (int r = 0; r < 4; ++r) {
-        int n = n0 + wv * 16 + 4 * g + r;
-        const float* wcr = w_cand + ((size_t)bs * Nn + n) * Dd;
-        const float* spr = surprise + ((size_t)bs * Nn + n) * Dd;
-        float pe = 0.f, ps = 0.f, wcv[8];
-        #pragma unroll
-        for (int dt = 0; dt < 8; ++dt) {
-            float wc = wcr[dt * 16 + q];
-            float rec = dacc[dt][r] * ivr[r];
-            float df = wc - rec;
-            pe += df * df;
-            float sv = spr[dt * 16 + q];
-            ps += sv * sv;
-            wcv[dt] = wc;
-        }
-        #pragma unroll
-        for (int off = 1; off < 16; off <<= 1) {
-            pe += __shfl_xor(pe, off);
-            ps += __shfl_xor(ps, off);
-        }
-        float novl = 0.5f * sqrtf(ps) + 0.5f * sqrtf(pe);
-        if (q == 0) stats[n] = novl;
-        float* der = delta_em + (((size_t)bs * Nn + n) * Bb + b) * Dd;
-        #pragma unroll
-        for (int dt = 0; dt < 8; ++dt) der[dt * 16 + q] = novl * wcv[dt];
-    }
-}
-
-__global__ __launch_bounds__(256) void k2b_pre(
-    const ushort_t* __restrict__ wnr, const ushort_t* __restrict__ wnT,
-    const ushort_t* __restrict__ Kbf,
-    const float* __restrict__ emK, const float* __restrict__ emV,
-    const float* __restrict__ emS, const float* __restrict__ emAge,
-    const float* __restrict__ g_em, const float* __restrict__ rtauw,
-    const float* __restrict__ nrmb,
-    float* __restrict__ newK, float* newV ,
-    float* __restrict__ newAge, float* __restrict__ newS, int mt_base)
-{
-    const int bs = blockIdx.z, b = blockIdx.y, mt = mt_base + blockIdx.x;
-    const int m0 = mt * 64;
-    const int tid = threadIdx.x;
-    const int wv = tid >> 6, l = tid & 63, g = l >> 4, q = l & 15;
-
-    __shared__ ushort_t klw[64][136];
-    __shared__ ushort_t vtw[128][72];
-    __shared__ float sh_rm[Nn], sh_f[Nn], sh_fn[Nn];
-
-    const float itw = 1.f / (softplusf(rtauw[b]) + 0.1f);
-    const float gv = g_em[bs * Bb + b];
-    const size_t pair = (size_t)(bs * Bb + b);
-    const float* stats = newV + pair * (size_t)(Mm * Dd) + 448 * Dd;
-
-    for (int i = tid; i < Nn; i += 256) {
-        float nv = stats[i];
-        float rm = stats[1024 + i];
-        float rs = stats[2048 + i];
-        float nr = nrmb[(size_t)bs * Nn + i];
-        sh_rm[i] = rm;
-        float f = nv / rs;
-        sh_f[i]  = f;
-        sh_fn[i] = f * nr;
-    }
-
-    const int myM = m0 + wv * 16 + q;
-    short8v kf[4];
-    {
-        const uint4* kr = (const uint4*)(Kbf + pair * 65536u + (size_t)myM * 128u);
-        #pragma unroll
-        for (int ck = 0; ck < 4; ++ck) {
-            union { short8v s; uint4 u; } r;
-            r.u = kr[ck * 4 + g];
-            kf[ck] = r.s;
-        }
-    }
-    const bool act = (emS[pair * Mm + myM] > 0.f);
-
-    const uint4* Wr = (const uint4*)(wnr + (size_t)bs * 131072u);
-    const uint4* Wt = (const uint4*)(wnT + (size_t)bs * 131072u);
-    uint4 wpf[4], tpf[4];
-    #pragma unroll
-    for (int j = 0; j < 4; ++j) { wpf[j] = Wr[tid + j * 256]; tpf[j] = Wt[tid + j * 256]; }
-
-    const f32x4 Z4 = {0.f, 0.f, 0.f, 0.f};
-    f32x4 uKacc[8], uVacc[8];
-    #pragma unroll
-    for (int dt = 0; dt < 8; ++dt) { uKacc[dt] = Z4; uVacc[dt] = Z4; }
-    float den = 0.f;
-
-    for (int nc = 0; nc < 16; ++nc) {
-        const int nb = nc * 64;
-        kwrite(klw, wpf, tid);
-        vwrite(vtw, tpf, tid);
-        __syncthreads();
-        if (nc < 15) {
-            #pragma unroll
-            for (int j = 0; j < 4; ++j) {
-                wpf[j] = Wr[(nc + 1) * 1024 + tid + j * 256];
-                tpf[j] = Wt[(nc + 1) * 1024 + tid + j * 256];
-            }
-        }
-
-        f32x4 sc[4];
-        #pragma unroll
-        for (int nt = 0; nt < 4; ++nt) {
-            f32x4 acc = Z4;
-            #pragma unroll
-            for (int ck = 0; ck < 4; ++ck)
-                acc = mfma16(read_kfrag(klw, nt, ck, g, q), kf[ck], acc);
-            sc[nt] = acc;
-        }
-        unsigned pwK[8], pwV[8];
-        #pragma unroll
-        for (int nt = 0; nt < 4; ++nt) {
-            float w0[4], w1[4];
-            #pragma unroll
-            for (int r = 0; r < 4; ++r) {
-                int nl = nb + nt * 16 + 4 * g + r;
-                float val = act ? sc[nt][r] * itw : NEGV;
-                float E = __expf(val - sh_rm[nl]);
-                float a = sh_f[nl] * E;
-                w0[r] = a;
-                w1[r] = sh_fn[nl] * E;
-                den += a;
-            }
-            pwK[nt * 2 + 0] = pack2bf(w0[0], w0[1]);
-            pwK[nt * 2 + 1] = pack2bf(w0[2], w0[3]);
-            pwV[nt * 2 + 0] = pack2bf(w1[0], w1[1]);
-            pwV[nt * 2 + 1] = pack2bf(w1[2], w1[3]);
-        }
-        union { short8v s; uint4 u; } paK0, paK1, paV0, paV1;
-        paK0.u = make_uint4(pwK[0], pwK[1], pwK[2], pwK[3]);
-        paK1.u = make_uint4(pwK[4], pwK[5], pwK[6], pwK[7]);
-        paV0.u = make_uint4(pwV[0], pwV[1], pwV[2], pwV[3]);
-        paV1.u = make_uint4(pwV[4], pwV[5], pwV[6], pwV[7]);
-        #pragma unroll
-        for (int dt = 0; dt < 8; ++dt) {
-            short8v b0 = read_vfrag(vtw, 0, dt, g, q);
-            short8v b1 = read_vfrag(vtw, 1, dt, g, q);
-            uKacc[dt] = mfma16(paK0.s, b0, uKacc[dt]);
-            uKacc[dt] = mfma16(paK1.s, b1, uKacc[dt]);
-            uVacc[dt] = mfma16(paV0.s, b0, uVacc[dt]);
-            uVacc[dt] = mfma16(paV1.s, b1, uVacc[dt]);
-        }
-        __syncthreads();
-    }
-
-    den += __shfl_xor(den, 16);
-    den += __shfl_xor(den, 32);
-    float invd = 1.f / fmaxf(den, 1e-8f);
-    float alpha = fminf(gv * den * (1.f / (float)Nn), 1.f);
-
-    float pr[4] = {0.f, 0.f, 0.f, 0.f};
-    #pragma unroll
-    for (int dt = 0; dt < 8; ++dt)
-        #pragma unroll
-        for (int r = 0; r < 4; ++r) { float u = uKacc[dt][r]; pr[r] += u * u; }
-    #pragma unroll
-    for (int r = 0; r < 4; ++r) {
-        #pragma unroll
-        for (int off = 1; off < 16; off <<= 1) pr[r] += __shfl_xor(pr[r], off);
-    }
-    float alr[4], idr[4], inr[4];
-    #pragma unroll
-    for (int r = 0; r < 4; ++r) {
-        alr[r] = __shfl(alpha, 4 * g + r);
-        idr[r] = __shfl(invd,  4 * g + r);
-        inr[r] = 1.f / fmaxf(sqrtf(pr[r]) * idr[r], 1e-12f);
-    }
-    #pragma unroll
-    for (int r = 0; r < 4; ++r) {
-        size_t rowoff = (pair * Mm + m0 + wv * 16 + 4 * g + r) * (size_t)Dd;
-        float a = alr[r], om = 1.f - a, id = idr[r], in = inr[r];
-        #pragma unroll
-        for (int dt = 0; dt < 8; ++dt) {
-            int d = dt * 16 + q;
-            float kv = emK[rowoff + d];
-            float vv = emV[rowoff + d];
-            newK[rowoff + d] = om * kv + a * uKacc[dt][r] * id * in;
-            newV[rowoff + d] = om * vv + a * uVacc[dt][r] * id;
-        }
-    }
-    if (q == 0) {
-        #pragma unroll
-        for (int r = 0; r < 4; ++r) {
-            int m = m0 + wv * 16 + 4 * g + r;
-            float a = alr[r];
-            float S = emS[pair * Mm + m];
-            newS[pair * Mm + m] = fminf(fmaxf(S + a, 0.f), 3.0f);
-            newAge[pair * Mm + m] = emAge[pair * Mm + m] * (1.f - a);
-        }
-    }
-}
-
-__global__ __launch_bounds__(256) void k1_fb(
-    const float* __restrict__ seed, const float* __restrict__ emK, const float* __restrict__ emV,
-    const float* __restrict__ emS, const float* __restrict__ w1, const float* __restrict__ w2,
-    const float* __restrict__ gb, const float* __restrict__ rtau, float* __restrict__ y_em)
-{
-    const int bs = blockIdx.z, b = blockIdx.y, n0 = blockIdx.x * 64;
-    const int tid = threadIdx.x;
-    const int wv = tid >> 6, l = tid & 63, g = l >> 4, q = l & 15;
-
-    __shared__ float yl[64][132];
-    __shared__ ushort_t kl[64][136];
-    __shared__ ushort_t vt[128][72];
-    __shared__ float sw1[Dd], sw2[Dd], sgb[Dd];
-
-    const float itau = 1.f / (softplusf(rtau[b]) + 0.1f);
-    const size_t pair = (size_t)(bs * Bb + b);
-    const float* Kb = emK + pair * (size_t)(Mm * Dd);
-    const float* Vb = emV + pair * (size_t)(Mm * Dd);
-
-    if (tid < Dd) {
-        sw1[tid] = w1[b * Dd + tid];
-        sw2[tid] = w2[b * Dd + tid];
-        sgb[tid] = gb[b * Dd + tid];
-    }
-    unsigned long long mlo = 0ull, mhi = 0ull;
-    {
-        const float4* sp = (const float4*)(emS + pair * Mm);
-        #pragma unroll 8
-        for (int t = 0; t < 32; ++t) {
-            float4 s = sp[t * 4 + g];
-            unsigned long long bits = (s.x > 0.f ? 1ull : 0ull) | (s.y > 0.f ? 2ull : 0ull)
-                                    | (s.z > 0.f ? 4ull : 0ull) | (s.w > 0.f ? 8ull : 0ull);
-            if (t < 16) mlo |= bits << (t * 4);
-            else        mhi |= bits << ((t - 16) * 4);
-        }
-    }
-    {
-        const float4* s4 = (const float4*)(seed + ((size_t)bs * Nn + n0) * Dd);
-        #pragma unroll
-        for (int it = 0; it < 8; ++it) {
-            int i = tid + it * 256;
-            *(float4*)&yl[i >> 5][(i & 31) * 4] = s4[i];
-        }
-    }
-    __syncthreads();
-
-    const f32x4 Z4 = {0.f, 0.f, 0.f, 0.f};
-
-    for (int step = 0; step < 2; ++step) {
-        short8v yf[4];
-        #pragma unroll
-        for (int ck = 0; ck < 4; ++ck) yf[ck] = build_yfrag(yl, wv * 16 + q, ck, g);
-
-        float m_run = NEGV, l_run = 0.f;
-        f32x4 dacc[8];
-        #pragma unroll
-        for (int dt = 0; dt < 8; ++dt) dacc[dt] = Z4;
-
-        for (int mc = 0; mc < 8; ++mc) {
-            stage_K64(Kb + (size_t)mc * 64 * Dd, kl, tid);
-            stage_VT(Vb + (size_t)mc * 64 * Dd, vt, tid);
-            __syncthreads();
-
-            f32x4 sc[4];
-            #pragma unroll
-            for (int mt = 0; mt < 4; ++mt) {
-                f32x4 acc = Z4;
-                #pragma unroll
-                for (int ck = 0; ck < 4; ++ck)
-                    acc = mfma16(read_kfrag(kl, mt, ck, g, q), yf[ck], acc);
-                sc[mt] = acc;
-            }
-            unsigned au = (unsigned)(((mc < 4) ? mlo : mhi) >> ((mc & 3) * 16)) & 0xFFFFu;
-            #pragma unroll
-            for (int mt = 0; mt < 4; ++mt)
-                #pragma unroll
-                for (int r = 0; r < 4; ++r)
-                    sc[mt][r] = ((au >> (mt * 4 + r)) & 1u) ? sc[mt][r] * itau : NEGV;
-            float cm = NEGV;
-            #pragma unroll
-            for (int mt = 0; mt < 4; ++mt)
-                #pragma unroll
-                for (int r = 0; r < 4; ++r) cm = fmaxf(cm, sc[mt][r]);
-            cm = fmaxf(cm, __shfl_xor(cm, 16));
-            cm = fmaxf(cm, __shfl_xor(cm, 32));
-            float mnew = fmaxf(m_run, cm);
-            float corr = __expf(m_run - mnew);
-            unsigned pw[8];
-            float psum = 0.f;
-            #pragma unroll
-            for (int mt = 0; mt < 4; ++mt)
-                #pragma unroll
-                for (int r = 0; r < 4; r += 2) {
-                    float e0 = __expf(sc[mt][r]     - mnew);
-                    float e1 = __expf(sc[mt][r + 1] - mnew);
-                    psum += e0 + e1;
-                    pw[mt * 2 + (r >> 1)] = pack2bf(e0, e1);
-                }
-            psum += __shfl_xor(psum, 16);
-            psum += __shfl_xor(psum, 32);
-            l_run = l_run * corr + psum;
-            m_run = mnew;
-            float cr[4];
-            #pragma unroll
-            for (int r = 0; r < 4; ++r) cr[r] = __shfl(corr, 4 * g + r);
-            #pragma unroll
-            for (int dt = 0; dt < 8; ++dt)
-                #pragma unroll
-                for (int r = 0; r < 4; ++r) dacc[dt][r] *= cr[r];
-            union { short8v s; uint4 u; } pa0, pa1;
-            pa0.u = make_uint4(pw[0], pw[1], pw[2], pw[3]);
-            pa1.u = make_uint4(pw[4], pw[5], pw[6], pw[7]);
-            #pragma unroll
-            for (int dt = 0; dt < 8; ++dt) {
-                f32x4 acc = dacc[dt];
-                acc = mfma16(pa0.s, read_vfrag(vt, 0, dt, g, q), acc);
-                acc = mfma16(pa1.s, read_vfrag(vt, 1, dt, g, q), acc);
-                dacc[dt] = acc;
-            }
-            __syncthreads();
-        }
-        float inv = (m_run != NEGV) ? 1.f / l_run : 0.f;
-        float ivr[4];
-        #pragma unroll
-        for (int r = 0; r < 4; ++r) ivr[r] = __shfl(inv, 4 * g + r);
-        #pragma unroll
-        for (int r = 0; r < 4; ++r) {
-            int row = wv * 16 + 4 * g + r;
-            #pragma unroll
-            for (int dt = 0; dt < 8; ++dt) {
-                int d = dt * 16 + q;
-                float del = dacc[dt][r] * ivr[r];
-                float y0 = yl[row][d];
-                float z = sw1[d] * y0 + sw2[d] * del + sgb[d];
-                float gte = 1.f / (1.f + __expf(-z));
-                yl[row][d] = y0 + gte * del;
-            }
-        }
-        __syncthreads();
-    }
-    #pragma unroll
-    for (int r16 = 0; r16 < 16; ++r16) {
-        int n = n0 + wv * 16 + r16;
-        float2 sv = *(const float2*)(seed + ((size_t)bs * Nn + n) * Dd + 2 * l);
-        float2 ov;
-        ov.x = yl[wv * 16 + r16][2 * l]     - sv.x;
-        ov.y = yl[wv * 16 + r16][2 * l + 1] - sv.y;
-        *(float2*)(y_em + (((size_t)bs * Nn + n) * Bb + b) * Dd + 2 * l) = ov;
-    }
-}
-
 __global__ __launch_bounds__(256) void k2a_fb(
     const float* __restrict__ w_cand, const float* __restrict__ surprise,
     const float* __restrict__ emK, const float* __restrict__ emV, const float* __restrict__ emS,
@@ -946,18 +936,8 @@
     const float* Vb = emV + pair * (size_t)(Mm * Dd);
     float* stats = newV + pair * (size_t)(Mm * Dd) + 448 * Dd;
 
-    unsigned long long mlo = 0ull, mhi = 0ull;
-    {
-        const float4* sp = (const float4*)(emS + pair * Mm);
-        #pragma unroll 8
-        for (int t = 0; t < 32; ++t) {
-            float4 s = sp[t * 4 + g];
-            unsigned long long bits = (s.x > 0.f ? 1ull : 0ull) | (s.y > 0.f ? 2ull : 0ull)
-                                    | (s.z > 0.f ? 4ull : 0ull) | (s.w > 0.f ? 8ull : 0ull);
-            if (t < 16) mlo |= bits << (t * 4);
-            else        mhi |= bits << ((t - 16) * 4);
-        }
-    }
+    unsigned long long mlo, mhi;
+    build_mask(emS, pair, g, mlo, mhi);
     {
         const float4* s4 = (const float4*)(w_cand + ((size_t)bs * Nn + n0) * Dd);
         #pragma unroll
@@ -1266,14 +1246,14 @@
     #pragma unroll
     for (int r = 0; r < 4; ++r) {
         size_t rowoff = (pair * Mm + m0 + wv * 16 + 4 * g + r) * (size_t)Dd;
-        float a = alr[r], om = 1.f - a, id = idr[r], in = inr[r];
+        float a = alr[r], om = 1.f - a, idv = idr[r], in = inr[r];
         #pragma unroll
         for (int dt = 0; dt < 8; ++dt) {
             int d = dt * 16 + q;
             float kv = emK[rowoff + d];
             float vv = emV[rowoff + d];
-            newK[rowoff + d] = om * kv + a * uKacc[dt][r] * id * in;
-            newV[rowoff + d] = om * vv + a * uVacc[dt][r] * id;
+            newK[rowoff + d] = om * kv + a * uKacc[dt][r] * idv * in;
+            newV[rowoff + d] = om * vv + a * uVacc[dt][r] * idv;
         }
     }
     if (q == 0) {
@@ -1333,7 +1313,6 @@
     float* newAge   = out + (size_t)25198592;
 
     dim3 blk(256);
-    dim3 g1(Nn / 64, Bb, BSz);
 
     const size_t WS_NEED = 21004288;
     if (d_ws != nullptr && ws_size >= WS_NEED) {
@@ -1343,18 +1322,20 @@
         ushort_t* wnT = wnr + (size_t)8 * 131072;
         float*    nrmb = (float*)(wnT + (size_t)8 * 131072);
 
-        k0kv<<<dim3(8, Bb, BSz), blk, 0, stream>>>(emK, emV, Kbf, Vtb);
-        k0w<<<dim3(16, BSz), blk, 0, stream>>>(w_cand, wnr, wnT, nrmb);
-        k1_pre<<<g1, blk, 0, stream>>>(seed, Kbf, Vtb, emS, w1, w2, gb, rtau, y_em);
-        k2a_pre<<<g1, blk, 0, stream>>>(w_cand, surprise, Kbf, Vtb, wnr, emS,
-                                        rtau, rtauw, delta_em, newV);
-        k2b_pre<<<dim3(7, Bb, BSz), blk, 0, stream>>>(wnr, wnT, Kbf, emK, emV, emS, emAge,
-                                                      g_em, rtauw, nrmb,
-                                                      newK, newV, newAge, newS, 0);
-        k2b_pre<<<dim3(1, Bb, BSz), blk, 0, stream>>>(wnr, wnT, Kbf, emK, emV, emS, emAge,
-                                                      g_em, rtauw, nrmb,
-                                                      newK, newV, newAge, newS, 7);
+        k0kv<<<dim3(512), blk, 0, stream>>>(emK, emV, Kbf, Vtb);
+        k0w<<<dim3(128), blk, 0, stream>>>(w_cand, wnr, wnT, nrmb);
+        k1_step<<<dim3(1024), blk, 0, stream>>>(seed, Kbf, Vtb, emS, w1, w2, gb, rtau, y_em, 0);
+        k1_step<<<dim3(1024), blk, 0, stream>>>(seed, Kbf, Vtb, emS, w1, w2, gb, rtau, y_em, 1);
+        k2a_pre<<<dim3(1024), blk, 0, stream>>>(w_cand, surprise, Kbf, Vtb, wnr, emS,
+                                                rtau, rtauw, delta_em, newV);
+        k2b_pre<<<dim3(448), blk, 0, stream>>>(wnr, wnT, Kbf, emK, emV, emS, emAge,
+                                               g_em, rtauw, nrmb,
+                                               newK, newV, newAge, newS, 0);
+        k2b_pre<<<dim3(64), blk, 0, stream>>>(wnr, wnT, Kbf, emK, emV, emS, emAge,
+                                              g_em, rtauw, nrmb,
+                                              newK, newV, newAge, newS, 1);
     } else {
+        dim3 g1(Nn / 64, Bb, BSz);
         k1_fb<<<g1, blk, 0, stream>>>(seed, emK, emV, emS, w1, w2, gb, rtau, y_em);
         k2a_fb<<<g1, blk, 0, stream>>>(w_cand, surprise, emK, emV, emS, rtau, rtauw,
                                        delta_em, newV);
```
